# Kernel tuning notes

Measured on AMD Instinct MI355X. Metric: run time of the kernel, lower is better.

The kernel has to match this reference:

```python
import jax, jax.numpy as jnp
import numpy as np

# dims: batch, sentences, p/q/a token lens, choices, hidden, selected sentences
B, N, P, Q, A, M, L, K = 32, 32, 64, 32, 24, 4, 768, 2
EPS = 1e-8


def _normalize(x):
    n = jnp.linalg.norm(x, axis=-1, keepdims=True)
    return x / jnp.maximum(n, EPS)


def setup_inputs() -> dict:
    key = jax.random.key(0)
    ks = jax.random.split(key, 16)
    w = lambda k, shape: jax.random.normal(k, shape, jnp.float32) * 0.02
    return {
        "H_p": jax.random.normal(ks[0], (B, N * P, L), jnp.float32),
        "H_q": jax.random.normal(ks[1], (B, Q, L), jnp.float32),
        "H_a": jax.random.normal(ks[2], (B, M * A, L), jnp.float32),
        "W5": w(ks[3], (L, L)),
        "W6": w(ks[4], ((M - 1) * L, L)),
        "W7": w(ks[5], (L, L)),
        "W8": w(ks[6], (L, L)),
        "b8": jnp.zeros((L,), jnp.float32),
        "W9": w(ks[7], (L, L)),
        "W10": w(ks[8], (L, L)),
        "W11": w(ks[9], (L, L)),
        "W12": w(ks[10], (L, L)),
        "W13": w(ks[11], (L, L)),
        "W14": w(ks[12], (L, L)),
        "b14": jnp.zeros((L,), jnp.float32),
        "V": w(ks[13], (3 * L, 1)),
    }


def reference(H_p, H_q, H_a, W5, W6, W7, W8, b8, W9, W10, W11, W12, W13, W14, b14, V):
    Bq = H_q.shape[0]
    Hp = H_p.reshape(Bq, N, P, L)   # (B, N, p, l)
    Ha = H_a.reshape(Bq, M, A, L)   # (B, m, a, l)

    # --- passage sentence selection (cosine scoring) ---
    # The torch code materializes O(B*m*N*a*p*l) repeated tensors; the math is just
    # pairwise cosine similarity -> max over passage tokens -> mean over a/q tokens.
    Pn, An, Qn = _normalize(Hp), _normalize(Ha), _normalize(H_q)
    sim_pa = jnp.einsum('bnpl,bmal->bmnap', Pn, An)  # (B, m, N, a, p)
    score_a = sim_pa.max(-1).mean(-1).sum(1)          # max over p, mean over a, sum over m -> (B, N)
    sim_pq = jnp.einsum('bnpl,bql->bnqp', Pn, Qn)     # (B, N, q, p)
    score_q = sim_pq.max(-1).mean(-1)                 # (B, N)
    score = score_a + score_q
    top_idx = jnp.argsort(-score, axis=-1)[:, :K]     # descending, top-K sentences
    H_p_s = jnp.take_along_axis(Hp, top_idx[:, :, None, None], axis=1).reshape(Bq, K * P, L)

    # --- answer option interaction ---
    H_o = []
    for i in range(M):
        Hi = Ha[:, i]                                  # (B, a, l)
        cache1 = Hi @ W5
        hats = []
        for j in range(M):
            if j != i:
                Hj = Ha[:, j]
                G = jax.nn.softmax(jnp.einsum('bal,bkl->bak', cache1, Hj), axis=-1)
                hats.append(jax.nn.relu(jnp.einsum('bak,bkl->bal', G, Hj)))
        bar = jnp.concatenate(hats, axis=-1) @ W6      # (B, a, l)
        g = jax.nn.sigmoid(bar @ W7 + bar @ W8 + b8)
        H_o.append(g * Hi + (1.0 - g) * bar)
    H_o = jnp.stack(H_o, axis=1)                       # (B, m, a, l)

    # --- bidirectional matching ---
    def match(Hx, Hy, Gxy_left, Gyx_left):
        Gxy = jax.nn.softmax(jnp.einsum('bxl,byl->bxy', Gxy_left, Hy), axis=-1)
        Gyx = jax.nn.softmax(jnp.einsum('byl,bxl->byx', Gyx_left, Hx), axis=-1)
        Ex = jnp.einsum('bxy,byl->bxl', Gxy, Hy)
        Ey = jnp.einsum('byx,bxl->byl', Gyx, Hx)
        Sxy = jax.nn.relu(Ex @ W11).max(1)             # (B, l)
        Syx = jax.nn.relu(Ey @ W12).max(1)             # (B, l)
        g = jax.nn.sigmoid(Sxy @ W13 + Syx @ W14 + b14)
        return g * Sxy + (1.0 - g) * Syx

    cache1 = H_p_s @ W9
    cache2 = H_q @ W9
    cache3 = H_q @ W10
    M_pq = match(H_p_s, H_q, cache1, cache3)
    C = []
    for i in range(M):
        Hoi = H_o[:, i]
        cache4 = Hoi @ W10
        M_po = match(H_p_s, Hoi, cache1, cache4)
        M_qo = match(H_q, Hoi, cache2, cache4)
        C.append(jnp.concatenate([M_pq, M_po, M_qo], axis=-1))
    C = jnp.stack(C, axis=1)                           # (B, m, 3l)
    logits = (C @ V).squeeze(-1)                       # (B, m)
    return jax.nn.log_softmax(logits, axis=-1)
```

## Files before the change

### kernel.cpp

```cpp
#include <hip/hip_runtime.h>
#include <math.h>


typedef __bf16 bf16x8 __attribute__((ext_vector_type(8)));
typedef float f32x4 __attribute__((ext_vector_type(4)));

__global__ __launch_bounds__(256) void prep_kernel(
    const float* __restrict__ W5, const float* __restrict__ W6,
    const float* __restrict__ W7, const float* __restrict__ W8,
    const float* __restrict__ W9, const float* __restrict__ W10,
    const float* __restrict__ W11, const float* __restrict__ W12,
    const float* __restrict__ W13, const float* __restrict__ W14,
    __bf16* __restrict__ W5t_h, __bf16* __restrict__ W5t_l,
    __bf16* __restrict__ WsQT_h, __bf16* __restrict__ WsQT_l,
    __bf16* __restrict__ W6t_h, __bf16* __restrict__ W6t_l,
    __bf16* __restrict__ W1112T, __bf16* __restrict__ W78t,
    __bf16* __restrict__ W1314t) {
    __shared__ float T[32][33];
    int blk = blockIdx.x;
    int job, rel;
    if (blk < 576) { job = 0; rel = blk; }
    else if (blk < 1728) { job = 1; rel = blk - 576; }
    else if (blk < 3456) { job = 2; rel = blk - 1728; }
    else if (blk < 4608) { job = 3; rel = blk - 3456; }
    else if (blk < 5184) { job = 4; rel = blk - 4608; }
    else { job = 5; rel = blk - 5184; }
    int KT = (job == 2) ? 72 : (job == 5) ? 48 : 24;
    int Kdim = KT * 32;
    int ntile = rel / KT, ktile = rel - ntile * KT;
    int k0 = ktile * 32, n0 = ntile * 32;
    int t = threadIdx.x, tx = t & 31, ty = t >> 5;
#pragma unroll
    for (int s = 0; s < 4; s++) {
        int k = k0 + ty + 8 * s;
        int n = n0 + tx;
        float v;
        switch (job) {
            case 0: v = W5[(long)k * 768 + n]; break;
            case 1: v = (n < 768) ? W9[(long)k * 768 + n] : W10[(long)k * 768 + n - 768]; break;
            case 2: v = W6[(long)k * 768 + n]; break;
            case 3: v = (n < 768) ? W11[(long)k * 768 + n] : W12[(long)k * 768 + n - 768]; break;
            case 4: v = W7[(long)k * 768 + n] + W8[(long)k * 768 + n]; break;
            default: v = (k < 768) ? W13[(long)k * 768 + n] : W14[(long)(k - 768) * 768 + n]; break;
        }
        T[ty + 8 * s][tx] = v;
    }
    __syncthreads();
#pragma unroll
    for (int s = 0; s < 4; s++) {
        int n = n0 + ty + 8 * s;
        int k = k0 + tx;
        float v = T[tx][ty + 8 * s];
        long o = (long)n * Kdim + k;
        __bf16 h = (__bf16)v;
        switch (job) {
            case 0: W5t_h[o] = h; W5t_l[o] = (__bf16)(v - (float)h); break;
            case 1: WsQT_h[o] = h; WsQT_l[o] = (__bf16)(v - (float)h); break;
            case 2: W6t_h[o] = h; W6t_l[o] = (__bf16)(v - (float)h); break;
            case 3: W1112T[o] = h; break;
            case 4: W78t[o] = h; break;
            default: W1314t[o] = h; break;
        }
    }
}

__global__ __launch_bounds__(256) void cvt2n_kernel(const float* __restrict__ src,
                                                    __bf16* __restrict__ h, __bf16* __restrict__ l,
                                                    float* __restrict__ rn) {
    long row = blockIdx.x;
    int t = threadIdx.x;
    const float* sr = src + row * 768;
    float ss = 0.f;
#pragma unroll
    for (int i = 0; i < 3; i++) {
        int idx = t + i * 256;
        float v = sr[idx];
        __bf16 hv = (__bf16)v;
        h[row * 768 + idx] = hv; l[row * 768 + idx] = (__bf16)(v - (float)hv);
        ss += v * v;
    }
    for (int o = 32; o; o >>= 1) ss += __shfl_xor(ss, o);
    __shared__ float red[4];
    if ((t & 63) == 0) red[t >> 6] = ss;
    __syncthreads();
    if (t == 0) rn[row] = 1.f / fmaxf(sqrtf(red[0] + red[1] + red[2] + red[3]), 1e-8f);
}

__global__ __launch_bounds__(256) void simmax_kernel(
    const float* __restrict__ Hp,
    const __bf16* __restrict__ Ha_h, const __bf16* __restrict__ Ha_l,
    const __bf16* __restrict__ Hq_h, const __bf16* __restrict__ Hq_l,
    const float* __restrict__ ra, const float* __restrict__ rq,
    float* __restrict__ amax) {
    constexpr int LDT = 72;
    __shared__ alignas(16) __bf16 Ah[64 * LDT];
    __shared__ alignas(16) __bf16 Al[64 * LDT];
    __shared__ alignas(16) __bf16 Bh[128 * LDT];
    __shared__ alignas(16) __bf16 Bl[128 * LDT];
    __shared__ float rp_lds[64];
    __shared__ float wred[4][128];
    int b = blockIdx.x >> 5, n = blockIdx.x & 31;
    int t = threadIdx.x;
    const float* Ap = Hp + ((long)b * 2048 + n * 64) * 768;
    int srow = t >> 2, kq = (t & 3) << 4;
    int brow = t >> 1, kh = (t & 1) << 5;
    const __bf16 *Bsh, *Bsl;
    if (brow < 96) {
        Bsh = Ha_h + (long)b * 73728 + (long)brow * 768;
        Bsl = Ha_l + (long)b * 73728 + (long)brow * 768;
    } else {
        Bsh = Hq_h + (long)b * 24576 + (long)(brow - 96) * 768;
        Bsl = Hq_l + (long)b * 24576 + (long)(brow - 96) * 768;
    }
    int w = t >> 6, l = t & 63;
    int fr = l & 15, g = l >> 4;
    int wr = w << 4;
    f32x4 acc[8] = {};
    float ss = 0.f;
    const float* Arow = Ap + (long)srow * 768 + kq;
    float4 av0, av1, av2, av3;
    bf16x8 vbh0, vbh1, vbh2, vbh3, vbl0, vbl1, vbl2, vbl3;
    auto LOADS = [&](int k0) {
        av0 = *(const float4*)(Arow + k0 + 0);
        av1 = *(const float4*)(Arow + k0 + 4);
        av2 = *(const float4*)(Arow + k0 + 8);
        av3 = *(const float4*)(Arow + k0 + 12);
        vbh0 = *(const bf16x8*)(Bsh + k0 + kh);
        vbh1 = *(const bf16x8*)(Bsh + k0 + kh + 8);
        vbh2 = *(const bf16x8*)(Bsh + k0 + kh + 16);
        vbh3 = *(const bf16x8*)(Bsh + k0 + kh + 24);
        vbl0 = *(const bf16x8*)(Bsl + k0 + kh);
        vbl1 = *(const bf16x8*)(Bsl + k0 + kh + 8);
        vbl2 = *(const bf16x8*)(Bsl + k0 + kh + 16);
        vbl3 = *(const bf16x8*)(Bsl + k0 + kh + 24);
    };
    LOADS(0);
    for (int k0 = 0; k0 < 768; k0 += 64) {
        float va[16];
        *(float4*)(va + 0) = av0; *(float4*)(va + 4) = av1;
        *(float4*)(va + 8) = av2; *(float4*)(va + 12) = av3;
        bf16x8 h0, h1, l0, l1;
#pragma unroll
        for (int i = 0; i < 8; i++) {
            float v = va[i]; __bf16 hv = (__bf16)v;
            h0[i] = hv; l0[i] = (__bf16)(v - (float)hv); ss += v * v;
            v = va[8 + i]; hv = (__bf16)v;
            h1[i] = hv; l1[i] = (__bf16)(v - (float)hv); ss += v * v;
        }
        bf16x8 sbh0 = vbh0, sbh1 = vbh1, sbh2 = vbh2, sbh3 = vbh3;
        bf16x8 sbl0 = vbl0, sbl1 = vbl1, sbl2 = vbl2, sbl3 = vbl3;
        __syncthreads();
        *(bf16x8*)(&Ah[srow * LDT + kq]) = h0;
        *(bf16x8*)(&Ah[srow * LDT + kq + 8]) = h1;
        *(bf16x8*)(&Al[srow * LDT + kq]) = l0;
        *(bf16x8*)(&Al[srow * LDT + kq + 8]) = l1;
        *(bf16x8*)(&Bh[brow * LDT + kh]) = sbh0;
        *(bf16x8*)(&Bh[brow * LDT + kh + 8]) = sbh1;
        *(bf16x8*)(&Bh[brow * LDT + kh + 16]) = sbh2;
        *(bf16x8*)(&Bh[brow * LDT + kh + 24]) = sbh3;
        *(bf16x8*)(&Bl[brow * LDT + kh]) = sbl0;
        *(bf16x8*)(&Bl[brow * LDT + kh + 8]) = sbl1;
        *(bf16x8*)(&Bl[brow * LDT + kh + 16]) = sbl2;
        *(bf16x8*)(&Bl[brow * LDT + kh + 24]) = sbl3;
        if (k0 + 64 < 768) LOADS(k0 + 64);
        __syncthreads();
#pragma unroll
        for (int sub = 0; sub < 2; sub++) {
            int kb = sub * 32 + g * 8;
            bf16x8 fah = *(const bf16x8*)(&Ah[(wr + fr) * LDT + kb]);
            bf16x8 fal = *(const bf16x8*)(&Al[(wr + fr) * LDT + kb]);
#pragma unroll
            for (int c = 0; c < 8; c++) {
                bf16x8 fbh = *(const bf16x8*)(&Bh[(c * 16 + fr) * LDT + kb]);
                bf16x8 fbl = *(const bf16x8*)(&Bl[(c * 16 + fr) * LDT + kb]);
                acc[c] = __builtin_amdgcn_mfma_f32_16x16x32_bf16(fah, fbh, acc[c], 0, 0, 0);
                acc[c] = __builtin_amdgcn_mfma_f32_16x16x32_bf16(fah, fbl, acc[c], 0, 0, 0);
                acc[c] = __builtin_amdgcn_mfma_f32_16x16x32_bf16(fal, fbh, acc[c], 0, 0, 0);
            }
        }
    }
    ss += __shfl_xor(ss, 1);
    ss += __shfl_xor(ss, 2);
    if ((t & 3) == 0) rp_lds[srow] = 1.f / fmaxf(sqrtf(ss), 1e-8f);
    __syncthreads();
    float rpv[4];
#pragma unroll
    for (int r = 0; r < 4; r++) rpv[r] = rp_lds[wr + g * 4 + r];
#pragma unroll
    for (int c = 0; c < 8; c++) {
        float mx = acc[c][0] * rpv[0];
        mx = fmaxf(mx, acc[c][1] * rpv[1]);
        mx = fmaxf(mx, acc[c][2] * rpv[2]);
        mx = fmaxf(mx, acc[c][3] * rpv[3]);
        mx = fmaxf(mx, __shfl_xor(mx, 16));
        mx = fmaxf(mx, __shfl_xor(mx, 32));
        if (g == 0) wred[w][c * 16 + fr] = mx;
    }
    __syncthreads();
    if (t < 128) {
        float m = fmaxf(fmaxf(wred[0][t], wred[1][t]), fmaxf(wred[2][t], wred[3][t]));
        float rc = (t < 96) ? ra[b * 96 + t] : rq[b * 32 + (t - 96)];
        amax[((long)b * 32 + n) * 128 + t] = m * rc;
    }
}

__global__ void score_top2_kernel(const float* __restrict__ amax, int* __restrict__ idx) {
    int b = blockIdx.x, t = threadIdx.x;
    __shared__ float sc[32];
    if (t < 32) {
        const float* am = amax + ((long)b * 32 + t) * 128;
        float sa = 0.f, sq = 0.f;
        for (int c = 0; c < 96; c++) sa += am[c];
        for (int c = 96; c < 128; c++) sq += am[c];
        sc[t] = sa / 24.f + sq / 32.f;
    }
    __syncthreads();
    if (t == 0) {
        float m0 = -1e30f; int i0 = 0;
        for (int n = 0; n < 32; n++) if (sc[n] > m0) { m0 = sc[n]; i0 = n; }
        float m1 = -1e30f; int i1 = 0;
        for (int n = 0; n < 32; n++) if (n != i0 && sc[n] > m1) { m1 = sc[n]; i1 = n; }
        idx[b * 2] = i0; idx[b * 2 + 1] = i1;
    }
}

__global__ void gather_kernel(const float* __restrict__ Hp, const int* __restrict__ idx,
                              __bf16* __restrict__ Hps_h, __bf16* __restrict__ Hps_l) {
    long i = (long)blockIdx.x * 256 + threadIdx.x;
    if (i >= (long)32 * 128 * 768) return;
    int l = (int)(i % 768);
    long r = i / 768;
    int x = (int)(r % 128); int b = (int)(r / 128);
    int k = x >> 6, p = x & 63;
    int n = idx[b * 2 + k];
    float v = Hp[((long)b * 2048 + n * 64 + p) * 768 + l];
    __bf16 h = (__bf16)v; Hps_h[i] = h; Hps_l[i] = (__bf16)(v - (float)h);
}

template <int BIASF, int BOUT>
__global__ __launch_bounds__(256) void mgemm_kernel(
    const __bf16* __restrict__ A, int Kdim, int Mtot,
    const __bf16* __restrict__ Wt, const float* __restrict__ bias,
    float* __restrict__ C, int ldc, __bf16* __restrict__ Cb) {
    constexpr int LDT = 80;
    __shared__ alignas(16) __bf16 As[64 * LDT];
    __shared__ alignas(16) __bf16 Bs[64 * LDT];
    int t = threadIdx.x;
    int rowBase = blockIdx.x << 6, colBase = blockIdx.y << 6;
    int srow = t >> 2, skof = (t & 3) << 3;
    int arow = rowBase + srow;
    bool aok = arow < Mtot;
    const __bf16* Ap = A + (long)(aok ? arow : rowBase) * Kdim + skof;
    const __bf16* Wp = Wt + (long)(colBase + srow) * Kdim + skof;
    int w = t >> 6, l = t & 63;
    int wr = (w >> 1) << 5, wc = (w & 1) << 5;
    int fr = l & 15, g = l >> 4;
    f32x4 acc[2][2] = {};
    int nk = Kdim >> 6;
    bf16x8 a0, a1, w0, w1;
    auto LOADM = [&]() {
        a0 = *(const bf16x8*)(Ap); a1 = *(const bf16x8*)(Ap + 32);
        w0 = *(const bf16x8*)(Wp); w1 = *(const bf16x8*)(Wp + 32);
        Ap += 64; Wp += 64;
    };
    LOADM();
    for (int ks = 0; ks < nk; ks++) {
        __syncthreads();
        *(bf16x8*)(&As[srow * LDT + skof]) = a0;
        *(bf16x8*)(&As[srow * LDT + 32 + skof]) = a1;
        *(bf16x8*)(&Bs[srow * LDT + skof]) = w0;
        *(bf16x8*)(&Bs[srow * LDT + 32 + skof]) = w1;
        if (ks + 1 < nk) LOADM();
        __syncthreads();
#pragma unroll
        for (int sub = 0; sub < 2; sub++) {
            int ko = sub * 32 + g * 8;
            bf16x8 fa0 = *(const bf16x8*)(&As[(wr + fr) * LDT + ko]);
            bf16x8 fa1 = *(const bf16x8*)(&As[(wr + 16 + fr) * LDT + ko]);
            bf16x8 fb0 = *(const bf16x8*)(&Bs[(wc + fr) * LDT + ko]);
            bf16x8 fb1 = *(const bf16x8*)(&Bs[(wc + 16 + fr) * LDT + ko]);
            acc[0][0] = __builtin_amdgcn_mfma_f32_16x16x32_bf16(fa0, fb0, acc[0][0], 0, 0, 0);
            acc[0][1] = __builtin_amdgcn_mfma_f32_16x16x32_bf16(fa0, fb1, acc[0][1], 0, 0, 0);
            acc[1][0] = __builtin_amdgcn_mfma_f32_16x16x32_bf16(fa1, fb0, acc[1][0], 0, 0, 0);
            acc[1][1] = __builtin_amdgcn_mfma_f32_16x16x32_bf16(fa1, fb1, acc[1][1], 0, 0, 0);
        }
    }
#pragma unroll
    for (int fi = 0; fi < 2; fi++)
#pragma unroll
    for (int fj = 0; fj < 2; fj++)
#pragma unroll
    for (int r = 0; r < 4; r++) {
        int row = rowBase + wr + fi * 16 + g * 4 + r;
        int col = colBase + wc + fj * 16 + (l & 15);
        if (row < Mtot) {
            float v = acc[fi][fj][r];
            if (BIASF) v += bias[col];
            if (BOUT == 0) C[(long)row * ldc + col] = v;
            else Cb[(long)row * ldc + col] = (__bf16)v;
        }
    }
}

__global__ __launch_bounds__(256) void mgemm_gate_kernel(
    const __bf16* __restrict__ A, const __bf16* __restrict__ Wt, const float* __restrict__ bias,
    const float* __restrict__ HaF, const float* __restrict__ barF,
    __bf16* __restrict__ Ho_h, __bf16* __restrict__ Ho_l) {
    constexpr int LDT = 80;
    constexpr int Kdim = 768;
    __shared__ alignas(16) __bf16 As[64 * LDT];
    __shared__ alignas(16) __bf16 Bs[64 * LDT];
    int t = threadIdx.x;
    int rowBase = blockIdx.x << 6, colBase = blockIdx.y << 6;
    int srow = t >> 2, skof = (t & 3) << 3;
    const __bf16* Ap = A + (long)(rowBase + srow) * Kdim + skof;
    const __bf16* Wp = Wt + (long)(colBase + srow) * Kdim + skof;
    int w = t >> 6, l = t & 63;
    int wr = (w >> 1) << 5, wc = (w & 1) << 5;
    int fr = l & 15, g = l >> 4;
    f32x4 acc[2][2] = {};
    bf16x8 a0, a1, w0, w1;
    auto LOADM = [&]() {
        a0 = *(const bf16x8*)(Ap); a1 = *(const bf16x8*)(Ap + 32);
        w0 = *(const bf16x8*)(Wp); w1 = *(const bf16x8*)(Wp + 32);
        Ap += 64; Wp += 64;
    };
    LOADM();
    for (int ks = 0; ks < 12; ks++) {
        __syncthreads();
        *(bf16x8*)(&As[srow * LDT + skof]) = a0;
        *(bf16x8*)(&As[srow * LDT + 32 + skof]) = a1;
        *(bf16x8*)(&Bs[srow * LDT + skof]) = w0;
        *(bf16x8*)(&Bs[srow * LDT + 32 + skof]) = w1;
        if (ks + 1 < 12) LOADM();
        __syncthreads();
#pragma unroll
        for (int sub = 0; sub < 2; sub++) {
            int ko = sub * 32 + g * 8;
            bf16x8 fa0 = *(const bf16x8*)(&As[(wr + fr) * LDT + ko]);
            bf16x8 fa1 = *(const bf16x8*)(&As[(wr + 16 + fr) * LDT + ko]);
            bf16x8 fb0 = *(const bf16x8*)(&Bs[(wc + fr) * LDT + ko]);
            bf16x8 fb1 = *(const bf16x8*)(&Bs[(wc + 16 + fr) * LDT + ko]);
            acc[0][0] = __builtin_amdgcn_mfma_f32_16x16x32_bf16(fa0, fb0, acc[0][0], 0, 0, 0);
            acc[0][1] = __builtin_amdgcn_mfma_f32_16x16x32_bf16(fa0, fb1, acc[0][1], 0, 0, 0);
            acc[1][0] = __builtin_amdgcn_mfma_f32_16x16x32_bf16(fa1, fb0, acc[1][0], 0, 0, 0);
            acc[1][1] = __builtin_amdgcn_mfma_f32_16x16x32_bf16(fa1, fb1, acc[1][1], 0, 0, 0);
        }
    }
#pragma unroll
    for (int fi = 0; fi < 2; fi++)
#pragma unroll
    for (int fj = 0; fj < 2; fj++)
#pragma unroll
    for (int r = 0; r < 4; r++) {
        int row = rowBase + wr + fi * 16 + g * 4 + r;
        int col = colBase + wc + fj * 16 + (l & 15);
        float v = acc[fi][fj][r] + bias[col];
        float gt = 1.f / (1.f + expf(-v));
        long o = (long)row * 768 + col;
        float hv = gt * HaF[o] + (1.f - gt) * barF[o];
        __bf16 hb = (__bf16)hv;
        Ho_h[o] = hb; Ho_l[o] = (__bf16)(hv - (float)hb);
    }
}

template <int OUT>
__global__ __launch_bounds__(256) void mgemm3_kernel(
    const __bf16* __restrict__ Ah, const __bf16* __restrict__ Al, int Kdim, int Mtot,
    const __bf16* __restrict__ Wh, const __bf16* __restrict__ Wl,
    float* __restrict__ C, int ldc, __bf16* __restrict__ Ch, __bf16* __restrict__ Cl) {
    constexpr int LDT = 80;
    __shared__ alignas(16) __bf16 Ahs[64 * LDT];
    __shared__ alignas(16) __bf16 Als[64 * LDT];
    __shared__ alignas(16) __bf16 Bhs[64 * LDT];
    __shared__ alignas(16) __bf16 Bls[64 * LDT];
    int t = threadIdx.x;
    int rowBase = blockIdx.x << 6, colBase = blockIdx.y << 6;
    int srow = t >> 2, skof = (t & 3) << 3;
    int arow = rowBase + srow;
    bool aok = arow < Mtot;
    long aoff = (long)(aok ? arow : rowBase) * Kdim + skof;
    long woff = (long)(colBase + srow) * Kdim + skof;
    const __bf16* Aph = Ah + aoff;
    const __bf16* Apl = Al + aoff;
    const __bf16* Wph = Wh + woff;
    const __bf16* Wpl = Wl + woff;
    int w = t >> 6, l = t & 63;
    int wr = (w >> 1) << 5, wc = (w & 1) << 5;
    int fr = l & 15, g = l >> 4;
    f32x4 acc[2][2] = {};
    int nk = Kdim >> 6;
    bf16x8 ah0, ah1, al0, al1, wh0, wh1, wl0, wl1;
    auto LOADM = [&]() {
        ah0 = *(const bf16x8*)(Aph); ah1 = *(const bf16x8*)(Aph + 32);
        al0 = *(const bf16x8*)(Apl); al1 = *(const bf16x8*)(Apl + 32);
        wh0 = *(const bf16x8*)(Wph); wh1 = *(const bf16x8*)(Wph + 32);
        wl0 = *(const bf16x8*)(Wpl); wl1 = *(const bf16x8*)(Wpl + 32);
        Aph += 64; Apl += 64; Wph += 64; Wpl += 64;
    };
    LOADM();
    for (int ks = 0; ks < nk; ks++) {
        __syncthreads();
        *(bf16x8*)(&Ahs[srow * LDT + skof]) = ah0; *(bf16x8*)(&Ahs[srow * LDT + 32 + skof]) = ah1;
        *(bf16x8*)(&Als[srow * LDT + skof]) = al0; *(bf16x8*)(&Als[srow * LDT + 32 + skof]) = al1;
        *(bf16x8*)(&Bhs[srow * LDT + skof]) = wh0; *(bf16x8*)(&Bhs[srow * LDT + 32 + skof]) = wh1;
        *(bf16x8*)(&Bls[srow * LDT + skof]) = wl0; *(bf16x8*)(&Bls[srow * LDT + 32 + skof]) = wl1;
        if (ks + 1 < nk) LOADM();
        __syncthreads();
#pragma unroll
        for (int sub = 0; sub < 2; sub++) {
            int ko = sub * 32 + g * 8;
            bf16x8 fah[2], fal[2], fbh[2], fbl[2];
            fah[0] = *(const bf16x8*)(&Ahs[(wr + fr) * LDT + ko]);
            fah[1] = *(const bf16x8*)(&Ahs[(wr + 16 + fr) * LDT + ko]);
            fal[0] = *(const bf16x8*)(&Als[(wr + fr) * LDT + ko]);
            fal[1] = *(const bf16x8*)(&Als[(wr + 16 + fr) * LDT + ko]);
            fbh[0] = *(const bf16x8*)(&Bhs[(wc + fr) * LDT + ko]);
            fbh[1] = *(const bf16x8*)(&Bhs[(wc + 16 + fr) * LDT + ko]);
            fbl[0] = *(const bf16x8*)(&Bls[(wc + fr) * LDT + ko]);
            fbl[1] = *(const bf16x8*)(&Bls[(wc + 16 + fr) * LDT + ko]);
#pragma unroll
            for (int i = 0; i < 2; i++)
#pragma unroll
            for (int j = 0; j < 2; j++) {
                acc[i][j] = __builtin_amdgcn_mfma_f32_16x16x32_bf16(fah[i], fbh[j], acc[i][j], 0, 0, 0);
                acc[i][j] = __builtin_amdgcn_mfma_f32_16x16x32_bf16(fah[i], fbl[j], acc[i][j], 0, 0, 0);
                acc[i][j] = __builtin_amdgcn_mfma_f32_16x16x32_bf16(fal[i], fbh[j], acc[i][j], 0, 0, 0);
            }
        }
    }
#pragma unroll
    for (int fi = 0; fi < 2; fi++)
#pragma unroll
    for (int fj = 0; fj < 2; fj++)
#pragma unroll
    for (int r = 0; r < 4; r++) {
        int row = rowBase + wr + fi * 16 + g * 4 + r;
        int col = colBase + wc + fj * 16 + (l & 15);
        if (row < Mtot) {
            float v = acc[fi][fj][r];
            long o = (long)row * ldc + col;
            if (OUT == 0) { C[o] = v; }
            else if (OUT == 1) { C[o] = v; Ch[o] = (__bf16)v; }
            else {
                __bf16 h = (__bf16)v;
                Ch[o] = h; Cl[o] = (__bf16)(v - (float)h);
            }
        }
    }
}

struct PXSeg { const __bf16 *Ah, *Al, *Wh, *Wl; __bf16 *Ch, *Cl; int Mtot, ldc, gx; };
struct PXArgs { PXSeg s[3]; };

__global__ __launch_bounds__(256) void projx_kernel(PXArgs args) {
    constexpr int LDT = 80;
    __shared__ alignas(16) __bf16 Ahs[64 * LDT];
    __shared__ alignas(16) __bf16 Als[64 * LDT];
    __shared__ alignas(16) __bf16 Bhs[64 * LDT];
    __shared__ alignas(16) __bf16 Bls[64 * LDT];
    int bid = blockIdx.x;
    int seg = (bid < 576) ? 0 : (bid < 960) ? 1 : 2;
    int rel = bid - ((seg == 0) ? 0 : (seg == 1) ? 576 : 960);
    PXSeg sg = args.s[seg];
    int rowBase = (rel % sg.gx) << 6, colBase = (rel / sg.gx) << 6;
    int t = threadIdx.x;
    int srow = t >> 2, skof = (t & 3) << 3;
    long aoff = (long)(rowBase + srow) * 768 + skof;
    long woff = (long)(colBase + srow) * 768 + skof;
    const __bf16* Aph = sg.Ah + aoff;
    const __bf16* Apl = sg.Al + aoff;
    const __bf16* Wph = sg.Wh + woff;
    const __bf16* Wpl = sg.Wl + woff;
    int w = t >> 6, l = t & 63;
    int wr = (w >> 1) << 5, wc = (w & 1) << 5;
    int fr = l & 15, g = l >> 4;
    f32x4 acc[2][2] = {};
    bf16x8 ah0, ah1, al0, al1, wh0, wh1, wl0, wl1;
    auto LOADM = [&]() {
        ah0 = *(const bf16x8*)(Aph); ah1 = *(const bf16x8*)(Aph + 32);
        al0 = *(const bf16x8*)(Apl); al1 = *(const bf16x8*)(Apl + 32);
        wh0 = *(const bf16x8*)(Wph); wh1 = *(const bf16x8*)(Wph + 32);
        wl0 = *(const bf16x8*)(Wpl); wl1 = *(const bf16x8*)(Wpl + 32);
        Aph += 64; Apl += 64; Wph += 64; Wpl += 64;
    };
    LOADM();
    for (int ks = 0; ks < 12; ks++) {
        __syncthreads();
        *(bf16x8*)(&Ahs[srow * LDT + skof]) = ah0; *(bf16x8*)(&Ahs[srow * LDT + 32 + skof]) = ah1;
        *(bf16x8*)(&Als[srow * LDT + skof]) = al0; *(bf16x8*)(&Als[srow * LDT + 32 + skof]) = al1;
        *(bf16x8*)(&Bhs[srow * LDT + skof]) = wh0; *(bf16x8*)(&Bhs[srow * LDT + 32 + skof]) = wh1;
        *(bf16x8*)(&Bls[srow * LDT + skof]) = wl0; *(bf16x8*)(&Bls[srow * LDT + 32 + skof]) = wl1;
        if (ks + 1 < 12) LOADM();
        __syncthreads();
#pragma unroll
        for (int sub = 0; sub < 2; sub++) {
            int ko = sub * 32 + g * 8;
            bf16x8 fah[2], fal[2], fbh[2], fbl[2];
            fah[0] = *(const bf16x8*)(&Ahs[(wr + fr) * LDT + ko]);
            fah[1] = *(const bf16x8*)(&Ahs[(wr + 16 + fr) * LDT + ko]);
            fal[0] = *(const bf16x8*)(&Als[(wr + fr) * LDT + ko]);
            fal[1] = *(const bf16x8*)(&Als[(wr + 16 + fr) * LDT + ko]);
            fbh[0] = *(const bf16x8*)(&Bhs[(wc + fr) * LDT + ko]);
            fbh[1] = *(const bf16x8*)(&Bhs[(wc + 16 + fr) * LDT + ko]);
            fbl[0] = *(const bf16x8*)(&Bls[(wc + fr) * LDT + ko]);
            fbl[1] = *(const bf16x8*)(&Bls[(wc + 16 + fr) * LDT + ko]);
#pragma unroll
            for (int i = 0; i < 2; i++)
#pragma unroll
            for (int j = 0; j < 2; j++) {
                acc[i][j] = __builtin_amdgcn_mfma_f32_16x16x32_bf16(fah[i], fbh[j], acc[i][j], 0, 0, 0);
                acc[i][j] = __builtin_amdgcn_mfma_f32_16x16x32_bf16(fah[i], fbl[j], acc[i][j], 0, 0, 0);
                acc[i][j] = __builtin_amdgcn_mfma_f32_16x16x32_bf16(fal[i], fbh[j], acc[i][j], 0, 0, 0);
            }
        }
    }
#pragma unroll
    for (int fi = 0; fi < 2; fi++)
#pragma unroll
    for (int fj = 0; fj < 2; fj++)
#pragma unroll
    for (int r = 0; r < 4; r++) {
        int row = rowBase + wr + fi * 16 + g * 4 + r;
        int col = colBase + wc + fj * 16 + (l & 15);
        if (row < sg.Mtot) {
            float v = acc[fi][fj][r];
            long o = (long)row * sg.ldc + col;
            __bf16 h = (__bf16)v;
            sg.Ch[o] = h; sg.Cl[o] = (__bf16)(v - (float)h);
        }
    }
}

struct PPSeg { const __bf16 *A, *Wt; __bf16* Cb; int Mtot, ldc, gx; };
struct PPArgs { PPSeg s[2]; };

__global__ __launch_bounds__(256) void projp_kernel(PPArgs args) {
    constexpr int LDT = 80;
    __shared__ alignas(16) __bf16 As[64 * LDT];
    __shared__ alignas(16) __bf16 Bs[64 * LDT];
    int bid = blockIdx.x;
    int seg = (bid < 384) ? 0 : 1;
    int rel = bid - ((seg == 0) ? 0 : 384);
    PPSeg sg = args.s[seg];
    int rowBase = (rel % sg.gx) << 6, colBase = (rel / sg.gx) << 6;
    int t = threadIdx.x;
    int srow = t >> 2, skof = (t & 3) << 3;
    const __bf16* Ap = sg.A + (long)(rowBase + srow) * 768 + skof;
    const __bf16* Wp = sg.Wt + (long)(colBase + srow) * 768 + skof;
    int w = t >> 6, l = t & 63;
    int wr = (w >> 1) << 5, wc = (w & 1) << 5;
    int fr = l & 15, g = l >> 4;
    f32x4 acc[2][2] = {};
    bf16x8 a0, a1, w0, w1;
    auto LOADM = [&]() {
        a0 = *(const bf16x8*)(Ap); a1 = *(const bf16x8*)(Ap + 32);
        w0 = *(const bf16x8*)(Wp); w1 = *(const bf16x8*)(Wp + 32);
        Ap += 64; Wp += 64;
    };
    LOADM();
    for (int ks = 0; ks < 12; ks++) {
        __syncthreads();
        *(bf16x8*)(&As[srow * LDT + skof]) = a0;
        *(bf16x8*)(&As[srow * LDT + 32 + skof]) = a1;
        *(bf16x8*)(&Bs[srow * LDT + skof]) = w0;
        *(bf16x8*)(&Bs[srow * LDT + 32 + skof]) = w1;
        if (ks + 1 < 12) LOADM();
        __syncthreads();
#pragma unroll
        for (int sub = 0; sub < 2; sub++) {
            int ko = sub * 32 + g * 8;
            bf16x8 fa0 = *(const bf16x8*)(&As[(wr + fr) * LDT + ko]);
            bf16x8 fa1 = *(const bf16x8*)(&As[(wr + 16 + fr) * LDT + ko]);
            bf16x8 fb0 = *(const bf16x8*)(&Bs[(wc + fr) * LDT + ko]);
            bf16x8 fb1 = *(const bf16x8*)(&Bs[(wc + 16 + fr) * LDT + ko]);
            acc[0][0] = __builtin_amdgcn_mfma_f32_16x16x32_bf16(fa0, fb0, acc[0][0], 0, 0, 0);
            acc[0][1] = __builtin_amdgcn_mfma_f32_16x16x32_bf16(fa0, fb1, acc[0][1], 0, 0, 0);
            acc[1][0] = __builtin_amdgcn_mfma_f32_16x16x32_bf16(fa1, fb0, acc[1][0], 0, 0, 0);
            acc[1][1] = __builtin_amdgcn_mfma_f32_16x16x32_bf16(fa1, fb1, acc[1][1], 0, 0, 0);
        }
    }
#pragma unroll
    for (int fi = 0; fi < 2; fi++)
#pragma unroll
    for (int fj = 0; fj < 2; fj++)
#pragma unroll
    for (int r = 0; r < 4; r++) {
        int row = rowBase + wr + fi * 16 + g * 4 + r;
        int col = colBase + wc + fj * 16 + (l & 15);
        if (row < sg.Mtot)
            sg.Cb[(long)row * sg.ldc + col] = (__bf16)acc[fi][fj][r];
    }
}

struct QHSeg {
    const __bf16 *GLh, *GLl, *HYh, *HYl;
    __bf16 *outH, *outL;
    long glB, hyB, oB;
};
struct QHArgs { QHSeg s[12]; };

__global__ __launch_bounds__(256) void qkh_kernel(QHArgs args) {
    constexpr int X = 24, Y = 24, XR = 32, YR = 32, LDT = 72;
    constexpr int YRp = YR + 1;
    constexpr int Ck = 32, Cpad = 40;
    constexpr int scPad = (XR * YRp * 4 + 15) & ~15;
    constexpr int btSz = 2 * 64 * Cpad * 2;
    constexpr int gOff = btSz;
    __shared__ alignas(16) char POOL[gOff + 2 * XR * Cpad * 2];
    __shared__ alignas(16) char POOL2[18432 - (gOff + 2 * XR * Cpad * 2)];
    (void)POOL2;
    __bf16* Ah_ = (__bf16*)POOL;
    __bf16* Al_ = Ah_ + XR * LDT;
    int seg = blockIdx.x >> 5, b = blockIdx.x & 31;
    QHSeg sg = args.s[seg];
    int t = threadIdx.x;
    __bf16* Bh_ = Ah_ + 2 * XR * LDT;
    __bf16* Bl_ = Bh_ + YR * LDT;
    float* sc   = (float*)POOL;
    float* invr = (float*)(POOL + scPad);
    __bf16* Bth = (__bf16*)POOL;
    __bf16* Btl = Bth + 64 * Cpad;
    __bf16* Gh  = (__bf16*)(POOL + gOff);
    __bf16* Gl  = Gh + XR * Cpad;
    int w = t >> 6, l = t & 63, fr = l & 15, g = l >> 4;
    const __bf16* GLbh = sg.GLh + (long)b * sg.glB;
    const __bf16* GLbl = sg.GLl + (long)b * sg.glB;
    const __bf16* HYbh = sg.HYh + (long)b * sg.hyB;
    const __bf16* HYbl = sg.HYl + (long)b * sg.hyB;
    f32x4 acc;
#pragma unroll
    for (int r = 0; r < 4; r++) acc[r] = 0.f;
    for (int k0 = 0; k0 < 768; k0 += 64) {
        __syncthreads();
        for (int v = t; v < (XR + YR) * 16; v += 256) {
            int row = v >> 4, sub = v & 15, hl = sub >> 3, k8 = (sub & 7) << 3;
            bf16x8 val = {};
            __bf16* dst;
            if (row < XR) {
                if (row < X)
                    val = *(const bf16x8*)((hl ? GLbl : GLbh) + (long)row * 768 + k0 + k8);
                dst = (hl ? Al_ : Ah_) + row * LDT + k8;
            } else {
                int r2 = row - XR;
                if (r2 < Y)
                    val = *(const bf16x8*)((hl ? HYbl : HYbh) + (long)r2 * 768 + k0 + k8);
                dst = (hl ? Bl_ : Bh_) + r2 * LDT + k8;
            }
            *(bf16x8*)dst = val;
        }
        __syncthreads();
#pragma unroll
        for (int sub = 0; sub < 2; sub++) {
            int kb = sub * 32 + g * 8;
            int xm = w >> 1, yc = w & 1;
            bf16x8 fah = *(const bf16x8*)(&Ah_[(xm * 16 + fr) * LDT + kb]);
            bf16x8 fal = *(const bf16x8*)(&Al_[(xm * 16 + fr) * LDT + kb]);
            bf16x8 fbh = *(const bf16x8*)(&Bh_[(yc * 16 + fr) * LDT + kb]);
            bf16x8 fbl = *(const bf16x8*)(&Bl_[(yc * 16 + fr) * LDT + kb]);
            acc = __builtin_amdgcn_mfma_f32_16x16x32_bf16(fah, fbh, acc, 0, 0, 0);
            acc = __builtin_amdgcn_mfma_f32_16x16x32_bf16(fah, fbl, acc, 0, 0, 0);
            acc = __builtin_amdgcn_mfma_f32_16x16x32_bf16(fal, fbh, acc, 0, 0, 0);
        }
    }
    __syncthreads();
    {
        int xm = w >> 1, yc = w & 1;
#pragma unroll
        for (int r = 0; r < 4; r++)
            sc[(xm * 16 + g * 4 + r) * YRp + yc * 16 + fr] = acc[r];
    }
    __syncthreads();
    {
        constexpr int TPR = 256 / XR;
        int row = t / TPR, sub = t & (TPR - 1);
        if (row < X) {
            float* sr = sc + row * YRp;
            float m = -1e30f;
            for (int c = sub; c < Y; c += TPR) m = fmaxf(m, sr[c]);
#pragma unroll
            for (int o = 1; o < TPR; o <<= 1) m = fmaxf(m, __shfl_xor(m, o));
            float s = 0.f;
            for (int c = sub; c < Y; c += TPR) { float e = expf(sr[c] - m); sr[c] = e; s += e; }
#pragma unroll
            for (int o = 1; o < TPR; o <<= 1) s += __shfl_xor(s, o);
            if (sub == 0) invr[row] = 1.f / s;
        }
    }
    __syncthreads();
    for (int idx = t; idx < XR * Ck; idx += 256) {
        int r = idx >> 5, c = idx & 31;
        float v = (r < X && c < Y) ? sc[r * YRp + c] * invr[r] : 0.f;
        __bf16 h = (__bf16)v;
        Gh[r * Cpad + c] = h; Gl[r * Cpad + c] = (__bf16)(v - (float)h);
    }
    int bl = t & 63, bc0 = t >> 6;
    for (int n0 = 0; n0 < 768; n0 += 64) {
        __syncthreads();
        for (int c = bc0; c < Ck; c += 4) {
            __bf16 hv = (__bf16)0.f, lv = (__bf16)0.f;
            if (c < Y) { hv = HYbh[(long)c * 768 + n0 + bl]; lv = HYbl[(long)c * 768 + n0 + bl]; }
            Bth[bl * Cpad + c] = hv; Btl[bl * Cpad + c] = lv;
        }
        __syncthreads();
        bf16x8 bh = *(const bf16x8*)(&Bth[(w * 16 + fr) * Cpad + g * 8]);
        bf16x8 blv = *(const bf16x8*)(&Btl[(w * 16 + fr) * Cpad + g * 8]);
        f32x4 a2[2] = {};
#pragma unroll
        for (int m = 0; m < 2; m++) {
            bf16x8 gah = *(const bf16x8*)(&Gh[(m * 16 + fr) * Cpad + g * 8]);
            bf16x8 gal = *(const bf16x8*)(&Gl[(m * 16 + fr) * Cpad + g * 8]);
            a2[m] = __builtin_amdgcn_mfma_f32_16x16x32_bf16(gah, bh, a2[m], 0, 0, 0);
            a2[m] = __builtin_amdgcn_mfma_f32_16x16x32_bf16(gal, bh, a2[m], 0, 0, 0);
            a2[m] = __builtin_amdgcn_mfma_f32_16x16x32_bf16(gah, blv, a2[m], 0, 0, 0);
        }
#pragma unroll
        for (int m = 0; m < 2; m++)
#pragma unroll
        for (int r = 0; r < 4; r++) {
            int row = m * 16 + g * 4 + r;
            if (row < X) {
                float v = fmaxf(a2[m][r], 0.f);
                __bf16 h = (__bf16)v;
                long o = (long)b * sg.oB + (long)row * 2304 + n0 + w * 16 + fr;
                sg.outH[o] = h; sg.outL[o] = (__bf16)(v - (float)h);
            }
        }
    }
}

struct QSSeg {
    const __bf16 *GLh, *GLl, *HYh, *HYl, *B;
    float* outF; __bf16* outH;
    long glB, hyB, bB;
    int ldGL, ldHY, ldB, shape;
};
struct QSArgs { QSSeg s[18]; };

template <int X, int Y>
__device__ __forceinline__ void qks_impl(char* POOL, const QSSeg& sg, int b, int t) {
    constexpr int XR = (X + 15) & ~15;
    constexpr int YR = (Y + 15) & ~15;
    constexpr int LDT = 72;
    constexpr int YC = YR / 16;
    constexpr int F = (XR / 16) * YC;
    constexpr int F4 = F / 4;
    constexpr int YRp = YR + 1;
    constexpr int Rk = XR;
    constexpr int Ck = (Y + 31) & ~31;
    constexpr int Cpad = Ck + 8;
    constexpr int NM = Rk / 16;
    constexpr int scPad = (XR * YRp * 4 + 15) & ~15;
    constexpr int invrEnd = scPad + 512;
    constexpr int btSz = 64 * Cpad * 2;
    constexpr int gOff = ((invrEnd > btSz ? invrEnd : btSz) + 15) & ~15;
    static_assert(gOff + 2 * Rk * Cpad * 2 <= 46080, "pool overflow");
    __bf16* Ah_ = (__bf16*)POOL;
    __bf16* Al_ = Ah_ + XR * LDT;
    __bf16* Bh_ = Ah_ + 2 * XR * LDT;
    __bf16* Bl_ = Bh_ + YR * LDT;
    float* sc   = (float*)POOL;
    float* invr = (float*)(POOL + scPad);
    __bf16* Bt  = (__bf16*)POOL;
    __bf16* Gh  = (__bf16*)(POOL + gOff);
    __bf16* Gl  = Gh + Rk * Cpad;
    int w = t >> 6, l = t & 63, fr = l & 15, g = l >> 4;
    const __bf16* GLbh = sg.GLh + (long)b * sg.glB;
    const __bf16* GLbl = sg.GLl + (long)b * sg.glB;
    const __bf16* HYbh = sg.HYh + (long)b * sg.hyB;
    const __bf16* HYbl = sg.HYl + (long)b * sg.hyB;
    f32x4 acc[F4] = {};
    for (int k0 = 0; k0 < 768; k0 += 64) {
        __syncthreads();
        for (int v = t; v < (XR + YR) * 16; v += 256) {
            int row = v >> 4, sub = v & 15, hl = sub >> 3, k8 = (sub & 7) << 3;
            bf16x8 val = {};
            __bf16* dst;
            if (row < XR) {
                if (row < X)
                    val = *(const bf16x8*)((hl ? GLbl : GLbh) + (long)row * sg.ldGL + k0 + k8);
                dst = (hl ? Al_ : Ah_) + row * LDT + k8;
            } else {
                int r2 = row - XR;
                if (r2 < Y)
                    val = *(const bf16x8*)((hl ? HYbl : HYbh) + (long)r2 * sg.ldHY + k0 + k8);
                dst = (hl ? Bl_ : Bh_) + r2 * LDT + k8;
            }
            *(bf16x8*)dst = val;
        }
        __syncthreads();
#pragma unroll
        for (int sub = 0; sub < 2; sub++) {
            int kb = sub * 32 + g * 8;
#pragma unroll
            for (int ff = 0; ff < F4; ff++) {
                int fidx = w + ff * 4;
                int xm = fidx / YC, yc = fidx % YC;
                bf16x8 fah = *(const bf16x8*)(&Ah_[(xm * 16 + fr) * LDT + kb]);
                bf16x8 fal = *(const bf16x8*)(&Al_[(xm * 16 + fr) * LDT + kb]);
                bf16x8 fbh = *(const bf16x8*)(&Bh_[(yc * 16 + fr) * LDT + kb]);
                bf16x8 fbl = *(const bf16x8*)(&Bl_[(yc * 16 + fr) * LDT + kb]);
                acc[ff] = __builtin_amdgcn_mfma_f32_16x16x32_bf16(fah, fbh, acc[ff], 0, 0, 0);
                acc[ff] = __builtin_amdgcn_mfma_f32_16x16x32_bf16(fah, fbl, acc[ff], 0, 0, 0);
                acc[ff] = __builtin_amdgcn_mfma_f32_16x16x32_bf16(fal, fbh, acc[ff], 0, 0, 0);
            }
        }
    }
    __syncthreads();
#pragma unroll
    for (int ff = 0; ff < F4; ff++) {
        int fidx = w + ff * 4;
        int xm = fidx / YC, yc = fidx % YC;
#pragma unroll
        for (int r = 0; r < 4; r++)
            sc[(xm * 16 + g * 4 + r) * YRp + yc * 16 + fr] = acc[ff][r];
    }
    __syncthreads();
    {
        constexpr int TPR = 256 / XR;
        int row = t / TPR, sub = t & (TPR - 1);
        if (row < X) {
            float* sr = sc + row * YRp;
            float m = -1e30f;
            for (int c = sub; c < Y; c += TPR) m = fmaxf(m, sr[c]);
#pragma unroll
            for (int o = 1; o < TPR; o <<= 1) m = fmaxf(m, __shfl_xor(m, o));
            float s = 0.f;
            for (int c = sub; c < Y; c += TPR) { float e = expf(sr[c] - m); sr[c] = e; s += e; }
#pragma unroll
            for (int o = 1; o < TPR; o <<= 1) s += __shfl_xor(s, o);
            if (sub == 0) invr[row] = 1.f / s;
        }
    }
    __syncthreads();
    for (int idx = t; idx < Rk * Ck; idx += 256) {
        int r = idx / Ck, c = idx - r * Ck;
        float v = (r < X && c < Y) ? sc[r * YRp + c] * invr[r] : 0.f;
        __bf16 h = (__bf16)v;
        Gh[r * Cpad + c] = h; Gl[r * Cpad + c] = (__bf16)(v - (float)h);
    }
    const __bf16* Bb = sg.B + (long)b * sg.bB;
    int bl = t & 63, bc0 = t >> 6;
    for (int n0 = 0; n0 < 768; n0 += 64) {
        __syncthreads();
        for (int c = bc0; c < Ck; c += 4) {
            __bf16 hv = (__bf16)0.f;
            if (c < Y) hv = Bb[(long)c * sg.ldB + n0 + bl];
            Bt[bl * Cpad + c] = hv;
        }
        __syncthreads();
        f32x4 a2[NM] = {};
#pragma unroll
        for (int ks = 0; ks < Ck; ks += 32) {
            bf16x8 bh = *(const bf16x8*)(&Bt[(w * 16 + fr) * Cpad + ks + g * 8]);
#pragma unroll
            for (int m = 0; m < NM; m++) {
                bf16x8 gah = *(const bf16x8*)(&Gh[(m * 16 + fr) * Cpad + ks + g * 8]);
                bf16x8 gal = *(const bf16x8*)(&Gl[(m * 16 + fr) * Cpad + ks + g * 8]);
                a2[m] = __builtin_amdgcn_mfma_f32_16x16x32_bf16(gah, bh, a2[m], 0, 0, 0);
                a2[m] = __builtin_amdgcn_mfma_f32_16x16x32_bf16(gal, bh, a2[m], 0, 0, 0);
            }
        }
        float mx = 0.f;
#pragma unroll
        for (int m = 0; m < NM; m++)
#pragma unroll
            for (int r = 0; r < 4; r++) mx = fmaxf(mx, a2[m][r]);
        mx = fmaxf(mx, __shfl_xor(mx, 16));
        mx = fmaxf(mx, __shfl_xor(mx, 32));
        if (g == 0) {
            int col = n0 + w * 16 + fr;
            sg.outF[(long)b * 1536 + col] = mx;
            sg.outH[(long)b * 1536 + col] = (__bf16)mx;
        }
    }
}

__global__ __launch_bounds__(256) void qks_kernel(QSArgs args) {
    __shared__ alignas(16) char POOL[46080];
    int seg = blockIdx.x >> 5, b = blockIdx.x & 31;
    QSSeg sg = args.s[seg];
    int t = threadIdx.x;
    switch (sg.shape) {
        case 1: qks_impl<128, 32>(POOL, sg, b, t); break;
        case 2: qks_impl<128, 24>(POOL, sg, b, t); break;
        case 3: qks_impl<32, 24>(POOL, sg, b, t); break;
        case 4: qks_impl<24, 32>(POOL, sg, b, t); break;
        case 5: qks_impl<32, 128>(POOL, sg, b, t); break;
        default: qks_impl<24, 128>(POOL, sg, b, t); break;
    }
}

__global__ __launch_bounds__(256) void logits_lsm_kernel(
    const float* __restrict__ S, const float* __restrict__ gts,
    const float* __restrict__ V, float* __restrict__ out) {
    int b = blockIdx.x;
    int t = threadIdx.x, i = t >> 6, lane = t & 63;
    int ms[3] = {0, 1 + i, 5 + i};
    float p = 0.f;
    for (int k = 0; k < 3; k++) {
        int m = ms[k];
        const float* Sr = S + (long)m * 49152 + (long)b * 1536;
        const float* gr = gts + ((long)m * 32 + b) * 768;
        const float* Vr = V + k * 768;
        for (int l = lane; l < 768; l += 64) {
            float g = 1.f / (1.f + expf(-gr[l]));
            p += (g * Sr[l] + (1.f - g) * Sr[768 + l]) * Vr[l];
        }
    }
    for (int o = 32; o; o >>= 1) p += __shfl_xor(p, o);
    __shared__ float lgs[4];
    if (lane == 0) lgs[i] = p;
    __syncthreads();
    if (t == 0) {
        float x0 = lgs[0], x1 = lgs[1], x2 = lgs[2], x3 = lgs[3];
        float m = fmaxf(fmaxf(x0, x1), fmaxf(x2, x3));
        float s = expf(x0 - m) + expf(x1 - m) + expf(x2 - m) + expf(x3 - m);
        float ls = m + logf(s);
        out[b * 4 + 0] = x0 - ls; out[b * 4 + 1] = x1 - ls;
        out[b * 4 + 2] = x2 - ls; out[b * 4 + 3] = x3 - ls;
    }
}

extern "C" void kernel_launch(void* const* d_in, const int* in_sizes, int n_in,
                              void* d_out, int out_size, void* d_ws, size_t ws_size,
                              hipStream_t stream) {
    const float* Hp  = (const float*)d_in[0];
    const float* Hq  = (const float*)d_in[1];
    const float* Ha  = (const float*)d_in[2];
    const float* W5  = (const float*)d_in[3];
    const float* W6  = (const float*)d_in[4];
    const float* W7  = (const float*)d_in[5];
    const float* W8  = (const float*)d_in[6];
    const float* b8  = (const float*)d_in[7];
    const float* W9  = (const float*)d_in[8];
    const float* W10 = (const float*)d_in[9];
    const float* W11 = (const float*)d_in[10];
    const float* W12 = (const float*)d_in[11];
    const float* W13 = (const float*)d_in[12];
    const float* W14 = (const float*)d_in[13];
    const float* b14 = (const float*)d_in[14];
    const float* V   = (const float*)d_in[15];
    float* out = (float*)d_out;
    (void)in_sizes; (void)n_in; (void)out_size; (void)ws_size;

    char* base = (char*)d_ws;
    size_t off = 0;
    auto take = [&](size_t bytes) { char* p = base + off; off += (bytes + 15) & ~15UL; return p; };

    __bf16* W5t_h  = (__bf16*)take(1179648);
    __bf16* W5t_l  = (__bf16*)take(1179648);
    __bf16* WsQT_h = (__bf16*)take(2359296);
    __bf16* WsQT_l = (__bf16*)take(2359296);
    __bf16* W6t_h  = (__bf16*)take(3538944);
    __bf16* W6t_l  = (__bf16*)take(3538944);
    __bf16* W1112T = (__bf16*)take(2359296);
    __bf16* W78t   = (__bf16*)take(1179648);
    __bf16* W1314t = (__bf16*)take(2359296);
    float* ra     = (float*)take(12288);
    float* rq     = (float*)take(4096);
    float* amax   = (float*)take(524288);
    int*   topidx = (int*)take(256);
    __bf16* Ha_h  = (__bf16*)take(4718592);
    __bf16* Ha_l  = (__bf16*)take(4718592);
    __bf16* Hq_h  = (__bf16*)take(1572864);
    __bf16* Hq_l  = (__bf16*)take(1572864);
    __bf16* Hps_h = (__bf16*)take(6291456);
    __bf16* Hps_l = (__bf16*)take(6291456);
    __bf16* C1_h  = (__bf16*)take(4718592);
    __bf16* C1_l  = (__bf16*)take(4718592);
    __bf16* HqS_h = (__bf16*)take(3145728);
    __bf16* HqS_l = (__bf16*)take(3145728);
    __bf16* c1_h  = (__bf16*)take(6291456);
    __bf16* c1_l  = (__bf16*)take(6291456);
    __bf16* c4_h  = (__bf16*)take(4718592);
    __bf16* c4_l  = (__bf16*)take(4718592);
    __bf16* Ho_h  = (__bf16*)take(4718592);
    __bf16* Ho_l  = (__bf16*)take(4718592);
    __bf16* hats_h = (__bf16*)take(14155776);
    __bf16* hats_l = (__bf16*)take(14155776);
    __bf16* bar_h  = (__bf16*)take(4718592);
    __bf16* HqS2_bf   = (__bf16*)take(3145728);
    __bf16* HpsW12_bf = (__bf16*)take(6291456);
    __bf16* HoW11_bf  = (__bf16*)take(4718592);
    __bf16* S_h    = (__bf16*)take(884736);
    float* bar  = (float*)take(9437184);
    float* S    = (float*)take(1769472);
    float* gts  = (float*)take(884736);

    dim3 blk(256);

    prep_kernel<<<6336, blk, 0, stream>>>(W5, W6, W7, W8, W9, W10, W11, W12, W13, W14,
                                          W5t_h, W5t_l, WsQT_h, WsQT_l, W6t_h, W6t_l,
                                          W1112T, W78t, W1314t);
    cvt2n_kernel<<<3072, blk, 0, stream>>>(Ha, Ha_h, Ha_l, ra);
    cvt2n_kernel<<<1024, blk, 0, stream>>>(Hq, Hq_h, Hq_l, rq);

    simmax_kernel<<<1024, blk, 0, stream>>>(Hp, Ha_h, Ha_l, Hq_h, Hq_l, ra, rq, amax);
    score_top2_kernel<<<32, dim3(64), 0, stream>>>(amax, topidx);
    gather_kernel<<<12288, blk, 0, stream>>>(Hp, topidx, Hps_h, Hps_l);

    {
        PXArgs pa{};
        pa.s[0] = { Ha_h, Ha_l, W5t_h, W5t_l, C1_h, C1_l, 3072, 768, 48 };
        pa.s[1] = { Hq_h, Hq_l, WsQT_h, WsQT_l, HqS_h, HqS_l, 1024, 1536, 16 };
        pa.s[2] = { Hps_h, Hps_l, WsQT_h, WsQT_l, c1_h, c1_l, 4096, 768, 64 };
        projx_kernel<<<1728, blk, 0, stream>>>(pa);
    }
    {
        PPArgs pa{};
        pa.s[0] = { Hq_h, W1112T, HqS2_bf, 1024, 1536, 16 };
        pa.s[1] = { Hps_h, W1112T + (long)768 * 768, HpsW12_bf, 4096, 768, 64 };
        projp_kernel<<<1152, blk, 0, stream>>>(pa);
    }

    {
        QHArgs qa{}; int si = 0;
        for (int i = 0; i < 4; i++) {
            int jj = 0;
            for (int j = 0; j < 4; j++) {
                if (j == i) continue;
                QHSeg& s = qa.s[si];
                s.GLh = C1_h + (long)i * 24 * 768; s.GLl = C1_l + (long)i * 24 * 768;
                s.HYh = Ha_h + (long)j * 24 * 768; s.HYl = Ha_l + (long)j * 24 * 768;
                s.outH = hats_h + (long)i * 24 * 2304 + jj * 768;
                s.outL = hats_l + (long)i * 24 * 2304 + jj * 768;
                s.glB = 73728; s.hyB = 73728; s.oB = 221184;
                si++; jj++;
            }
        }
        qkh_kernel<<<12 * 32, blk, 0, stream>>>(qa);
    }
    mgemm3_kernel<1><<<dim3(48, 12), blk, 0, stream>>>(hats_h, hats_l, 2304, 3072, W6t_h, W6t_l, bar, 768, bar_h, nullptr);
    mgemm_gate_kernel<<<dim3(48, 12), blk, 0, stream>>>(bar_h, W78t, b8, Ha, bar, Ho_h, Ho_l);
    mgemm3_kernel<2><<<dim3(48, 12), blk, 0, stream>>>(Ho_h, Ho_l, 768, 3072, WsQT_h + (long)768 * 768, WsQT_l + (long)768 * 768, nullptr, 768, c4_h, c4_l);
    mgemm_kernel<0, 1><<<dim3(48, 12), blk, 0, stream>>>(Ho_h, 768, 3072, W1112T, nullptr, nullptr, 768, HoW11_bf);

    {
        QSArgs qa{};
        auto set = [&](int k, const __bf16* GLh, const __bf16* GLl, long glB, int ldGL,
                       const __bf16* HYh, const __bf16* HYl, long hyB, int ldHY,
                       const __bf16* B, long bB, int ldB,
                       float* oF, __bf16* oH, int shape) {
            QSSeg& s = qa.s[k];
            s.GLh = GLh; s.GLl = GLl; s.HYh = HYh; s.HYl = HYl; s.B = B;
            s.outF = oF; s.outH = oH;
            s.glB = glB; s.hyB = hyB; s.bB = bB;
            s.ldGL = ldGL; s.ldHY = ldHY; s.ldB = ldB; s.shape = shape;
        };
        set(0, c1_h, c1_l, 98304, 768, Hq_h, Hq_l, 24576, 768,
            HqS2_bf, 49152, 1536, S, S_h, 1);
        for (int i = 0; i < 4; i++) {
            set(1 + i, c1_h, c1_l, 98304, 768,
                Ho_h + (long)i * 24 * 768, Ho_l + (long)i * 24 * 768, 73728, 768,
                HoW11_bf + (long)i * 24 * 768, 73728, 768,
                S + (long)(1 + i) * 49152, S_h + (long)(1 + i) * 49152, 2);
            set(5 + i, HqS_h, HqS_l, 49152, 1536,
                Ho_h + (long)i * 24 * 768, Ho_l + (long)i * 24 * 768, 73728, 768,
                HoW11_bf + (long)i * 24 * 768, 73728, 768,
                S + (long)(5 + i) * 49152, S_h + (long)(5 + i) * 49152, 3);
            set(9 + i, c4_h + (long)i * 24 * 768, c4_l + (long)i * 24 * 768, 73728, 768,
                Hq_h, Hq_l, 24576, 768,
                HqS2_bf + 768, 49152, 1536,
                S + (long)(5 + i) * 49152 + 768, S_h + (long)(5 + i) * 49152 + 768, 4);
        }
        set(13, HqS_h + 768, HqS_l + 768, 49152, 1536, Hps_h, Hps_l, 98304, 768,
            HpsW12_bf, 98304, 768, S + 768, S_h + 768, 5);
        for (int i = 0; i < 4; i++)
            set(14 + i, c4_h + (long)i * 24 * 768, c4_l + (long)i * 24 * 768, 73728, 768,
                Hps_h, Hps_l, 98304, 768,
                HpsW12_bf, 98304, 768,
                S + (long)(1 + i) * 49152 + 768, S_h + (long)(1 + i) * 49152 + 768, 6);
        qks_kernel<<<18 * 32, blk, 0, stream>>>(qa);
    }

    mgemm_kernel<1, 0><<<dim3(5, 12), blk, 0, stream>>>(S_h, 1536, 288, W1314t, b14, gts, 768, nullptr);

    logits_lsm_kernel<<<32, blk, 0, stream>>>(S, gts, V, out);
}
```

Baseline: 442.1 us.

## Enlarge projection GEMM tiles to 128x128 with 4x4 MFMA fragments per wave

Replaces the 64x64-tile projection and split-bf16 GEMM kernels with 128x128-tile versions in which each wave computes a 64x64 sub-tile (4x4 MFMA fragments). The aim is more operand reuse per LDS load and less global traffic per output. It also merges the two cvt2n launches into one and simplifies the qkh shared-memory declaration. In exchange there are far fewer blocks (e.g. 144 instead of 576), which can underfill a 256-CU GPU, and register pressure per wave is higher. The row-bounds checks are dropped, so every M must be a multiple of 128.

```diff
diff --git a/kernel.cpp b/kernel.cpp
--- a/kernel.cpp
+++ b/kernel.cpp
@@ -4,6 +4,8 @@
 
 typedef __bf16 bf16x8 __attribute__((ext_vector_type(8)));
 typedef float f32x4 __attribute__((ext_vector_type(4)));
+
+#define MFMA __builtin_amdgcn_mfma_f32_16x16x32_bf16
 
 __global__ __launch_bounds__(256) void prep_kernel(
     const float* __restrict__ W5, const float* __restrict__ W6,
@@ -64,10 +66,15 @@
     }
 }
 
-__global__ __launch_bounds__(256) void cvt2n_kernel(const float* __restrict__ src,
-                                                    __bf16* __restrict__ h, __bf16* __restrict__ l,
-                                                    float* __restrict__ rn) {
+__global__ __launch_bounds__(256) void cvt2n_kernel(
+    const float* __restrict__ Ha, __bf16* __restrict__ Ha_h, __bf16* __restrict__ Ha_l,
+    float* __restrict__ ra,
+    const float* __restrict__ Hq, __bf16* __restrict__ Hq_h, __bf16* __restrict__ Hq_l,
+    float* __restrict__ rq) {
     long row = blockIdx.x;
+    const float* src; __bf16 *h, *l; float* rn;
+    if (row < 3072) { src = Ha; h = Ha_h; l = Ha_l; rn = ra; }
+    else { row -= 3072; src = Hq; h = Hq_h; l = Hq_l; rn = rq; }
     int t = threadIdx.x;
     const float* sr = src + row * 768;
     float ss = 0.f;
@@ -173,9 +180,9 @@
             for (int c = 0; c < 8; c++) {
                 bf16x8 fbh = *(const bf16x8*)(&Bh[(c * 16 + fr) * LDT + kb]);
                 bf16x8 fbl = *(const bf16x8*)(&Bl[(c * 16 + fr) * LDT + kb]);
-                acc[c] = __builtin_amdgcn_mfma_f32_16x16x32_bf16(fah, fbh, acc[c], 0, 0, 0);
-                acc[c] = __builtin_amdgcn_mfma_f32_16x16x32_bf16(fah, fbl, acc[c], 0, 0, 0);
-                acc[c] = __builtin_amdgcn_mfma_f32_16x16x32_bf16(fal, fbh, acc[c], 0, 0, 0);
+                acc[c] = MFMA(fah, fbh, acc[c], 0, 0, 0);
+                acc[c] = MFMA(fah, fbl, acc[c], 0, 0, 0);
+                acc[c] = MFMA(fal, fbh, acc[c], 0, 0, 0);
             }
         }
     }
@@ -235,6 +242,189 @@
     int n = idx[b * 2 + k];
     float v = Hp[((long)b * 2048 + n * 64 + p) * 768 + l];
     __bf16 h = (__bf16)v; Hps_h[i] = h; Hps_l[i] = (__bf16)(v - (float)h);
+}
+
+template <int OUT>
+__device__ __forceinline__ void mg3b_body(
+    const __bf16* __restrict__ Ah, const __bf16* __restrict__ Al, int Kdim,
+    const __bf16* __restrict__ Wh, const __bf16* __restrict__ Wl,
+    float* __restrict__ C, int ldc, __bf16* __restrict__ Ch, __bf16* __restrict__ Cl,
+    int rowBase, int colBase, int t,
+    __bf16* Ahs, __bf16* Als, __bf16* Bhs, __bf16* Bls) {
+    constexpr int LDT = 40;
+    int srow = t >> 1, skof = (t & 1) << 4;
+    long aoff = (long)(rowBase + srow) * Kdim + skof;
+    long woff = (long)(colBase + srow) * Kdim + skof;
+    const __bf16* Aph = Ah + aoff;
+    const __bf16* Apl = Al + aoff;
+    const __bf16* Wph = Wh + woff;
+    const __bf16* Wpl = Wl + woff;
+    int w = t >> 6, l = t & 63;
+    int wr = (w >> 1) << 6, wc = (w & 1) << 6;
+    int fr = l & 15, g = l >> 4;
+    f32x4 acc[4][4] = {};
+    int nk = Kdim >> 5;
+    bf16x8 rah0, rah1, ral0, ral1, rwh0, rwh1, rwl0, rwl1;
+    auto LOADM = [&]() {
+        rah0 = *(const bf16x8*)(Aph); rah1 = *(const bf16x8*)(Aph + 8);
+        ral0 = *(const bf16x8*)(Apl); ral1 = *(const bf16x8*)(Apl + 8);
+        rwh0 = *(const bf16x8*)(Wph); rwh1 = *(const bf16x8*)(Wph + 8);
+        rwl0 = *(const bf16x8*)(Wpl); rwl1 = *(const bf16x8*)(Wpl + 8);
+        Aph += 32; Apl += 32; Wph += 32; Wpl += 32;
+    };
+    LOADM();
+    for (int ks = 0; ks < nk; ks++) {
+        __syncthreads();
+        *(bf16x8*)(&Ahs[srow * LDT + skof]) = rah0; *(bf16x8*)(&Ahs[srow * LDT + skof + 8]) = rah1;
+        *(bf16x8*)(&Als[srow * LDT + skof]) = ral0; *(bf16x8*)(&Als[srow * LDT + skof + 8]) = ral1;
+        *(bf16x8*)(&Bhs[srow * LDT + skof]) = rwh0; *(bf16x8*)(&Bhs[srow * LDT + skof + 8]) = rwh1;
+        *(bf16x8*)(&Bls[srow * LDT + skof]) = rwl0; *(bf16x8*)(&Bls[srow * LDT + skof + 8]) = rwl1;
+        if (ks + 1 < nk) LOADM();
+        __syncthreads();
+        int kb = g * 8;
+        bf16x8 fah[4], fal[4], fbh[4], fbl[4];
+#pragma unroll
+        for (int i = 0; i < 4; i++) {
+            fah[i] = *(const bf16x8*)(&Ahs[(wr + i * 16 + fr) * LDT + kb]);
+            fal[i] = *(const bf16x8*)(&Als[(wr + i * 16 + fr) * LDT + kb]);
+            fbh[i] = *(const bf16x8*)(&Bhs[(wc + i * 16 + fr) * LDT + kb]);
+            fbl[i] = *(const bf16x8*)(&Bls[(wc + i * 16 + fr) * LDT + kb]);
+        }
+#pragma unroll
+        for (int i = 0; i < 4; i++)
+#pragma unroll
+        for (int j = 0; j < 4; j++) {
+            acc[i][j] = MFMA(fah[i], fbh[j], acc[i][j], 0, 0, 0);
+            acc[i][j] = MFMA(fah[i], fbl[j], acc[i][j], 0, 0, 0);
+            acc[i][j] = MFMA(fal[i], fbh[j], acc[i][j], 0, 0, 0);
+        }
+    }
+#pragma unroll
+    for (int fi = 0; fi < 4; fi++)
+#pragma unroll
+    for (int fj = 0; fj < 4; fj++)
+#pragma unroll
+    for (int r = 0; r < 4; r++) {
+        int row = rowBase + wr + fi * 16 + g * 4 + r;
+        int col = colBase + wc + fj * 16 + fr;
+        float v = acc[fi][fj][r];
+        long o = (long)row * ldc + col;
+        if (OUT == 1) { C[o] = v; Ch[o] = (__bf16)v; }
+        else {
+            __bf16 h = (__bf16)v;
+            Ch[o] = h; Cl[o] = (__bf16)(v - (float)h);
+        }
+    }
+}
+
+template <int OUT>
+__global__ __launch_bounds__(256) void mgemm3b_kernel(
+    const __bf16* __restrict__ Ah, const __bf16* __restrict__ Al, int Kdim,
+    const __bf16* __restrict__ Wh, const __bf16* __restrict__ Wl,
+    float* __restrict__ C, int ldc, __bf16* __restrict__ Ch, __bf16* __restrict__ Cl) {
+    __shared__ alignas(16) __bf16 Ahs[128 * 40];
+    __shared__ alignas(16) __bf16 Als[128 * 40];
+    __shared__ alignas(16) __bf16 Bhs[128 * 40];
+    __shared__ alignas(16) __bf16 Bls[128 * 40];
+    mg3b_body<OUT>(Ah, Al, Kdim, Wh, Wl, C, ldc, Ch, Cl,
+                   blockIdx.x << 7, blockIdx.y << 7, threadIdx.x, Ahs, Als, Bhs, Bls);
+}
+
+struct PXSeg { const __bf16 *Ah, *Al, *Wh, *Wl; __bf16 *Ch, *Cl; int ldc, gx; };
+struct PXArgs { PXSeg s[3]; };
+
+__global__ __launch_bounds__(256) void projxb_kernel(PXArgs args) {
+    __shared__ alignas(16) __bf16 Ahs[128 * 40];
+    __shared__ alignas(16) __bf16 Als[128 * 40];
+    __shared__ alignas(16) __bf16 Bhs[128 * 40];
+    __shared__ alignas(16) __bf16 Bls[128 * 40];
+    int bid = blockIdx.x;
+    int seg = (bid < 144) ? 0 : (bid < 240) ? 1 : 2;
+    int rel = bid - ((seg == 0) ? 0 : (seg == 1) ? 144 : 240);
+    PXSeg sg = args.s[seg];
+    int rowBase = (rel % sg.gx) << 7, colBase = (rel / sg.gx) << 7;
+    mg3b_body<2>(sg.Ah, sg.Al, 768, sg.Wh, sg.Wl, nullptr, sg.ldc, sg.Ch, sg.Cl,
+                 rowBase, colBase, threadIdx.x, Ahs, Als, Bhs, Bls);
+}
+
+__device__ __forceinline__ void mgb_body(
+    const __bf16* __restrict__ A, int Kdim, const __bf16* __restrict__ Wt,
+    __bf16* __restrict__ Cb, int ldc,
+    int rowBase, int colBase, int t, __bf16* As, __bf16* Bs) {
+    constexpr int LDT = 72;
+    int srow = t >> 1, skof = (t & 1) << 5;
+    const __bf16* Ap = A + (long)(rowBase + srow) * Kdim + skof;
+    const __bf16* Wp = Wt + (long)(colBase + srow) * Kdim + skof;
+    int w = t >> 6, l = t & 63;
+    int wr = (w >> 1) << 6, wc = (w & 1) << 6;
+    int fr = l & 15, g = l >> 4;
+    f32x4 acc[4][4] = {};
+    int nk = Kdim >> 6;
+    bf16x8 ra0, ra1, ra2, ra3, rw0, rw1, rw2, rw3;
+    auto LOADM = [&]() {
+        ra0 = *(const bf16x8*)(Ap);      ra1 = *(const bf16x8*)(Ap + 8);
+        ra2 = *(const bf16x8*)(Ap + 16); ra3 = *(const bf16x8*)(Ap + 24);
+        rw0 = *(const bf16x8*)(Wp);      rw1 = *(const bf16x8*)(Wp + 8);
+        rw2 = *(const bf16x8*)(Wp + 16); rw3 = *(const bf16x8*)(Wp + 24);
+        Ap += 64; Wp += 64;
+    };
+    LOADM();
+    for (int ks = 0; ks < nk; ks++) {
+        __syncthreads();
+        *(bf16x8*)(&As[srow * LDT + skof]) = ra0;      *(bf16x8*)(&As[srow * LDT + skof + 8]) = ra1;
+        *(bf16x8*)(&As[srow * LDT + skof + 16]) = ra2; *(bf16x8*)(&As[srow * LDT + skof + 24]) = ra3;
+        *(bf16x8*)(&Bs[srow * LDT + skof]) = rw0;      *(bf16x8*)(&Bs[srow * LDT + skof + 8]) = rw1;
+        *(bf16x8*)(&Bs[srow * LDT + skof + 16]) = rw2; *(bf16x8*)(&Bs[srow * LDT + skof + 24]) = rw3;
+        if (ks + 1 < nk) LOADM();
+        __syncthreads();
+#pragma unroll
+        for (int sub = 0; sub < 2; sub++) {
+            int kb = sub * 32 + g * 8;
+            bf16x8 fa[4], fb[4];
+#pragma unroll
+            for (int i = 0; i < 4; i++) {
+                fa[i] = *(const bf16x8*)(&As[(wr + i * 16 + fr) * LDT + kb]);
+                fb[i] = *(const bf16x8*)(&Bs[(wc + i * 16 + fr) * LDT + kb]);
+            }
+#pragma unroll
+            for (int i = 0; i < 4; i++)
+#pragma unroll
+            for (int j = 0; j < 4; j++)
+                acc[i][j] = MFMA(fa[i], fb[j], acc[i][j], 0, 0, 0);
+        }
+    }
+#pragma unroll
+    for (int fi = 0; fi < 4; fi++)
+#pragma unroll
+    for (int fj = 0; fj < 4; fj++)
+#pragma unroll
+    for (int r = 0; r < 4; r++) {
+        int row = rowBase + wr + fi * 16 + g * 4 + r;
+        int col = colBase + wc + fj * 16 + fr;
+        Cb[(long)row * ldc + col] = (__bf16)acc[fi][fj][r];
+    }
+}
+
+__global__ __launch_bounds__(256) void mgemmb_kernel(
+    const __bf16* __restrict__ A, int Kdim, const __bf16* __restrict__ Wt,
+    __bf16* __restrict__ Cb, int ldc) {
+    __shared__ alignas(16) __bf16 As[128 * 72];
+    __shared__ alignas(16) __bf16 Bs[128 * 72];
+    mgb_body(A, Kdim, Wt, Cb, ldc, blockIdx.x << 7, blockIdx.y << 7, threadIdx.x, As, Bs);
+}
+
+struct PPSeg { const __bf16 *A, *Wt; __bf16* Cb; int ldc, gx; };
+struct PPArgs { PPSeg s[2]; };
+
+__global__ __launch_bounds__(256) void projpb_kernel(PPArgs args) {
+    __shared__ alignas(16) __bf16 As[128 * 72];
+    __shared__ alignas(16) __bf16 Bs[128 * 72];
+    int bid = blockIdx.x;
+    int seg = (bid < 96) ? 0 : 1;
+    int rel = bid - ((seg == 0) ? 0 : 96);
+    PPSeg sg = args.s[seg];
+    int rowBase = (rel % sg.gx) << 7, colBase = (rel / sg.gx) << 7;
+    mgb_body(sg.A, 768, sg.Wt, sg.Cb, sg.ldc, rowBase, colBase, threadIdx.x, As, Bs);
 }
 
 template <int BIASF, int BOUT>
@@ -279,10 +469,10 @@
             bf16x8 fa1 = *(const bf16x8*)(&As[(wr + 16 + fr) * LDT + ko]);
             bf16x8 fb0 = *(const bf16x8*)(&Bs[(wc + fr) * LDT + ko]);
             bf16x8 fb1 = *(const bf16x8*)(&Bs[(wc + 16 + fr) * LDT + ko]);
-            acc[0][0] = __builtin_amdgcn_mfma_f32_16x16x32_bf16(fa0, fb0, acc[0][0], 0, 0, 0);
-            acc[0][1] = __builtin_amdgcn_mfma_f32_16x16x32_bf16(fa0, fb1, acc[0][1], 0, 0, 0);
-            acc[1][0] = __builtin_amdgcn_mfma_f32_16x16x32_bf16(fa1, fb0, acc[1][0], 0, 0, 0);
-            acc[1][1] = __builtin_amdgcn_mfma_f32_16x16x32_bf16(fa1, fb1, acc[1][1], 0, 0, 0);
+            acc[0][0] = MFMA(fa0, fb0, acc[0][0], 0, 0, 0);
+            acc[0][1] = MFMA(fa0, fb1, acc[0][1], 0, 0, 0);
+            acc[1][0] = MFMA(fa1, fb0, acc[1][0], 0, 0, 0);
+            acc[1][1] = MFMA(fa1, fb1, acc[1][1], 0, 0, 0);
         }
     }
 #pragma unroll
@@ -341,10 +531,10 @@
             bf16x8 fa1 = *(const bf16x8*)(&As[(wr + 16 + fr) * LDT + ko]);
             bf16x8 fb0 = *(const bf16x8*)(&Bs[(wc + fr) * LDT + ko]);
             bf16x8 fb1 = *(const bf16x8*)(&Bs[(wc + 16 + fr) * LDT + ko]);
-            acc[0][0] = __builtin_amdgcn_mfma_f32_16x16x32_bf16(fa0, fb0, acc[0][0], 0, 0, 0);
-            acc[0][1] = __builtin_amdgcn_mfma_f32_16x16x32_bf16(fa0, fb1, acc[0][1], 0, 0, 0);
-            acc[1][0] = __builtin_amdgcn_mfma_f32_16x16x32_bf16(fa1, fb0, acc[1][0], 0, 0, 0);
-            acc[1][1] = __builtin_amdgcn_mfma_f32_16x16x32_bf16(fa1, fb1, acc[1][1], 0, 0, 0);
+            acc[0][0] = MFMA(fa0, fb0, acc[0][0], 0, 0, 0);
+            acc[0][1] = MFMA(fa0, fb1, acc[0][1], 0, 0, 0);
+            acc[1][0] = MFMA(fa1, fb0, acc[1][0], 0, 0, 0);
+            acc[1][1] = MFMA(fa1, fb1, acc[1][1], 0, 0, 0);
         }
     }
 #pragma unroll
@@ -364,235 +554,6 @@
     }
 }
 
-template <int OUT>
-__global__ __launch_bounds__(256) void mgemm3_kernel(
-    const __bf16* __restrict__ Ah, const __bf16* __restrict__ Al, int Kdim, int Mtot,
-    const __bf16* __restrict__ Wh, const __bf16* __restrict__ Wl,
-    float* __restrict__ C, int ldc, __bf16* __restrict__ Ch, __bf16* __restrict__ Cl) {
-    constexpr int LDT = 80;
-    __shared__ alignas(16) __bf16 Ahs[64 * LDT];
-    __shared__ alignas(16) __bf16 Als[64 * LDT];
-    __shared__ alignas(16) __bf16 Bhs[64 * LDT];
-    __shared__ alignas(16) __bf16 Bls[64 * LDT];
-    int t = threadIdx.x;
-    int rowBase = blockIdx.x << 6, colBase = blockIdx.y << 6;
-    int srow = t >> 2, skof = (t & 3) << 3;
-    int arow = rowBase + srow;
-    bool aok = arow < Mtot;
-    long aoff = (long)(aok ? arow : rowBase) * Kdim + skof;
-    long woff = (long)(colBase + srow) * Kdim + skof;
-    const __bf16* Aph = Ah + aoff;
-    const __bf16* Apl = Al + aoff;
-    const __bf16* Wph = Wh + woff;
-    const __bf16* Wpl = Wl + woff;
-    int w = t >> 6, l = t & 63;
-    int wr = (w >> 1) << 5, wc = (w & 1) << 5;
-    int fr = l & 15, g = l >> 4;
-    f32x4 acc[2][2] = {};
-    int nk = Kdim >> 6;
-    bf16x8 ah0, ah1, al0, al1, wh0, wh1, wl0, wl1;
-    auto LOADM = [&]() {
-        ah0 = *(const bf16x8*)(Aph); ah1 = *(const bf16x8*)(Aph + 32);
-        al0 = *(const bf16x8*)(Apl); al1 = *(const bf16x8*)(Apl + 32);
-        wh0 = *(const bf16x8*)(Wph); wh1 = *(const bf16x8*)(Wph + 32);
-        wl0 = *(const bf16x8*)(Wpl); wl1 = *(const bf16x8*)(Wpl + 32);
-        Aph += 64; Apl += 64; Wph += 64; Wpl += 64;
-    };
-    LOADM();
-    for (int ks = 0; ks < nk; ks++) {
-        __syncthreads();
-        *(bf16x8*)(&Ahs[srow * LDT + skof]) = ah0; *(bf16x8*)(&Ahs[srow * LDT + 32 + skof]) = ah1;
-        *(bf16x8*)(&Als[srow * LDT + skof]) = al0; *(bf16x8*)(&Als[srow * LDT + 32 + skof]) = al1;
-        *(bf16x8*)(&Bhs[srow * LDT + skof]) = wh0; *(bf16x8*)(&Bhs[srow * LDT + 32 + skof]) = wh1;
-        *(bf16x8*)(&Bls[srow * LDT + skof]) = wl0; *(bf16x8*)(&Bls[srow * LDT + 32 + skof]) = wl1;
-        if (ks + 1 < nk) LOADM();
-        __syncthreads();
-#pragma unroll
-        for (int sub = 0; sub < 2; sub++) {
-            int ko = sub * 32 + g * 8;
-            bf16x8 fah[2], fal[2], fbh[2], fbl[2];
-            fah[0] = *(const bf16x8*)(&Ahs[(wr + fr) * LDT + ko]);
-            fah[1] = *(const bf16x8*)(&Ahs[(wr + 16 + fr) * LDT + ko]);
-            fal[0] = *(const bf16x8*)(&Als[(wr + fr) * LDT + ko]);
-            fal[1] = *(const bf16x8*)(&Als[(wr + 16 + fr) * LDT + ko]);
-            fbh[0] = *(const bf16x8*)(&Bhs[(wc + fr) * LDT + ko]);
-            fbh[1] = *(const bf16x8*)(&Bhs[(wc + 16 + fr) * LDT + ko]);
-            fbl[0] = *(const bf16x8*)(&Bls[(wc + fr) * LDT + ko]);
-            fbl[1] = *(const bf16x8*)(&Bls[(wc + 16 + fr) * LDT + ko]);
-#pragma unroll
-            for (int i = 0; i < 2; i++)
-#pragma unroll
-            for (int j = 0; j < 2; j++) {
-                acc[i][j] = __builtin_amdgcn_mfma_f32_16x16x32_bf16(fah[i], fbh[j], acc[i][j], 0, 0, 0);
-                acc[i][j] = __builtin_amdgcn_mfma_f32_16x16x32_bf16(fah[i], fbl[j], acc[i][j], 0, 0, 0);
-                acc[i][j] = __builtin_amdgcn_mfma_f32_16x16x32_bf16(fal[i], fbh[j], acc[i][j], 0, 0, 0);
-            }
-        }
-    }
-#pragma unroll
-    for (int fi = 0; fi < 2; fi++)
-#pragma unroll
-    for (int fj = 0; fj < 2; fj++)
-#pragma unroll
-    for (int r = 0; r < 4; r++) {
-        int row = rowBase + wr + fi * 16 + g * 4 + r;
-        int col = colBase + wc + fj * 16 + (l & 15);
-        if (row < Mtot) {
-            float v = acc[fi][fj][r];
-            long o = (long)row * ldc + col;
-            if (OUT == 0) { C[o] = v; }
-            else if (OUT == 1) { C[o] = v; Ch[o] = (__bf16)v; }
-            else {
-                __bf16 h = (__bf16)v;
-                Ch[o] = h; Cl[o] = (__bf16)(v - (float)h);
-            }
-        }
-    }
-}
-
-struct PXSeg { const __bf16 *Ah, *Al, *Wh, *Wl; __bf16 *Ch, *Cl; int Mtot, ldc, gx; };
-struct PXArgs { PXSeg s[3]; };
-
-__global__ __launch_bounds__(256) void projx_kernel(PXArgs args) {
-    constexpr int LDT = 80;
-    __shared__ alignas(16) __bf16 Ahs[64 * LDT];
-    __shared__ alignas(16) __bf16 Als[64 * LDT];
-    __shared__ alignas(16) __bf16 Bhs[64 * LDT];
-    __shared__ alignas(16) __bf16 Bls[64 * LDT];
-    int bid = blockIdx.x;
-    int seg = (bid < 576) ? 0 : (bid < 960) ? 1 : 2;
-    int rel = bid - ((seg == 0) ? 0 : (seg == 1) ? 576 : 960);
-    PXSeg sg = args.s[seg];
-    int rowBase = (rel % sg.gx) << 6, colBase = (rel / sg.gx) << 6;
-    int t = threadIdx.x;
-    int srow = t >> 2, skof = (t & 3) << 3;
-    long aoff = (long)(rowBase + srow) * 768 + skof;
-    long woff = (long)(colBase + srow) * 768 + skof;
-    const __bf16* Aph = sg.Ah + aoff;
-    const __bf16* Apl = sg.Al + aoff;
-    const __bf16* Wph = sg.Wh + woff;
-    const __bf16* Wpl = sg.Wl + woff;
-    int w = t >> 6, l = t & 63;
-    int wr = (w >> 1) << 5, wc = (w & 1) << 5;
-    int fr = l & 15, g = l >> 4;
-    f32x4 acc[2][2] = {};
-    bf16x8 ah0, ah1, al0, al1, wh0, wh1, wl0, wl1;
-    auto LOADM = [&]() {
-        ah0 = *(const bf16x8*)(Aph); ah1 = *(const bf16x8*)(Aph + 32);
-        al0 = *(const bf16x8*)(Apl); al1 = *(const bf16x8*)(Apl + 32);
-        wh0 = *(const bf16x8*)(Wph); wh1 = *(const bf16x8*)(Wph + 32);
-        wl0 = *(const bf16x8*)(Wpl); wl1 = *(const bf16x8*)(Wpl + 32);
-        Aph += 64; Apl += 64; Wph += 64; Wpl += 64;
-    };
-    LOADM();
-    for (int ks = 0; ks < 12; ks++) {
-        __syncthreads();
-        *(bf16x8*)(&Ahs[srow * LDT + skof]) = ah0; *(bf16x8*)(&Ahs[srow * LDT + 32 + skof]) = ah1;
-        *(bf16x8*)(&Als[srow * LDT + skof]) = al0; *(bf16x8*)(&Als[srow * LDT + 32 + skof]) = al1;
-        *(bf16x8*)(&Bhs[srow * LDT + skof]) = wh0; *(bf16x8*)(&Bhs[srow * LDT + 32 + skof]) = wh1;
-        *(bf16x8*)(&Bls[srow * LDT + skof]) = wl0; *(bf16x8*)(&Bls[srow * LDT + 32 + skof]) = wl1;
-        if (ks + 1 < 12) LOADM();
-        __syncthreads();
-#pragma unroll
-        for (int sub = 0; sub < 2; sub++) {
-            int ko = sub * 32 + g * 8;
-            bf16x8 fah[2], fal[2], fbh[2], fbl[2];
-            fah[0] = *(const bf16x8*)(&Ahs[(wr + fr) * LDT + ko]);
-            fah[1] = *(const bf16x8*)(&Ahs[(wr + 16 + fr) * LDT + ko]);
-            fal[0] = *(const bf16x8*)(&Als[(wr + fr) * LDT + ko]);
-            fal[1] = *(const bf16x8*)(&Als[(wr + 16 + fr) * LDT + ko]);
-            fbh[0] = *(const bf16x8*)(&Bhs[(wc + fr) * LDT + ko]);
-            fbh[1] = *(const bf16x8*)(&Bhs[(wc + 16 + fr) * LDT + ko]);
-            fbl[0] = *(const bf16x8*)(&Bls[(wc + fr) * LDT + ko]);
-            fbl[1] = *(const bf16x8*)(&Bls[(wc + 16 + fr) * LDT + ko]);
-#pragma unroll
-            for (int i = 0; i < 2; i++)
-#pragma unroll
-            for (int j = 0; j < 2; j++) {
-                acc[i][j] = __builtin_amdgcn_mfma_f32_16x16x32_bf16(fah[i], fbh[j], acc[i][j], 0, 0, 0);
-                acc[i][j] = __builtin_amdgcn_mfma_f32_16x16x32_bf16(fah[i], fbl[j], acc[i][j], 0, 0, 0);
-                acc[i][j] = __builtin_amdgcn_mfma_f32_16x16x32_bf16(fal[i], fbh[j], acc[i][j], 0, 0, 0);
-            }
-        }
-    }
-#pragma unroll
-    for (int fi = 0; fi < 2; fi++)
-#pragma unroll
-    for (int fj = 0; fj < 2; fj++)
-#pragma unroll
-    for (int r = 0; r < 4; r++) {
-        int row = rowBase + wr + fi * 16 + g * 4 + r;
-        int col = colBase + wc + fj * 16 + (l & 15);
-        if (row < sg.Mtot) {
-            float v = acc[fi][fj][r];
-            long o = (long)row * sg.ldc + col;
-            __bf16 h = (__bf16)v;
-            sg.Ch[o] = h; sg.Cl[o] = (__bf16)(v - (float)h);
-        }
-    }
-}
-
-struct PPSeg { const __bf16 *A, *Wt; __bf16* Cb; int Mtot, ldc, gx; };
-struct PPArgs { PPSeg s[2]; };
-
-__global__ __launch_bounds__(256) void projp_kernel(PPArgs args) {
-    constexpr int LDT = 80;
-    __shared__ alignas(16) __bf16 As[64 * LDT];
-    __shared__ alignas(16) __bf16 Bs[64 * LDT];
-    int bid = blockIdx.x;
-    int seg = (bid < 384) ? 0 : 1;
-    int rel = bid - ((seg == 0) ? 0 : 384);
-    PPSeg sg = args.s[seg];
-    int rowBase = (rel % sg.gx) << 6, colBase = (rel / sg.gx) << 6;
-    int t = threadIdx.x;
-    int srow = t >> 2, skof = (t & 3) << 3;
-    const __bf16* Ap = sg.A + (long)(rowBase + srow) * 768 + skof;
-    const __bf16* Wp = sg.Wt + (long)(colBase + srow) * 768 + skof;
-    int w = t >> 6, l = t & 63;
-    int wr = (w >> 1) << 5, wc = (w & 1) << 5;
-    int fr = l & 15, g = l >> 4;
-    f32x4 acc[2][2] = {};
-    bf16x8 a0, a1, w0, w1;
-    auto LOADM = [&]() {
-        a0 = *(const bf16x8*)(Ap); a1 = *(const bf16x8*)(Ap + 32);
-        w0 = *(const bf16x8*)(Wp); w1 = *(const bf16x8*)(Wp + 32);
-        Ap += 64; Wp += 64;
-    };
-    LOADM();
-    for (int ks = 0; ks < 12; ks++) {
-        __syncthreads();
-        *(bf16x8*)(&As[srow * LDT + skof]) = a0;
-        *(bf16x8*)(&As[srow * LDT + 32 + skof]) = a1;
-        *(bf16x8*)(&Bs[srow * LDT + skof]) = w0;
-        *(bf16x8*)(&Bs[srow * LDT + 32 + skof]) = w1;
-        if (ks + 1 < 12) LOADM();
-        __syncthreads();
-#pragma unroll
-        for (int sub = 0; sub < 2; sub++) {
-            int ko = sub * 32 + g * 8;
-            bf16x8 fa0 = *(const bf16x8*)(&As[(wr + fr) * LDT + ko]);
-            bf16x8 fa1 = *(const bf16x8*)(&As[(wr + 16 + fr) * LDT + ko]);
-            bf16x8 fb0 = *(const bf16x8*)(&Bs[(wc + fr) * LDT + ko]);
-            bf16x8 fb1 = *(const bf16x8*)(&Bs[(wc + 16 + fr) * LDT + ko]);
-            acc[0][0] = __builtin_amdgcn_mfma_f32_16x16x32_bf16(fa0, fb0, acc[0][0], 0, 0, 0);
-            acc[0][1] = __builtin_amdgcn_mfma_f32_16x16x32_bf16(fa0, fb1, acc[0][1], 0, 0, 0);
-            acc[1][0] = __builtin_amdgcn_mfma_f32_16x16x32_bf16(fa1, fb0, acc[1][0], 0, 0, 0);
-            acc[1][1] = __builtin_amdgcn_mfma_f32_16x16x32_bf16(fa1, fb1, acc[1][1], 0, 0, 0);
-        }
-    }
-#pragma unroll
-    for (int fi = 0; fi < 2; fi++)
-#pragma unroll
-    for (int fj = 0; fj < 2; fj++)
-#pragma unroll
-    for (int r = 0; r < 4; r++) {
-        int row = rowBase + wr + fi * 16 + g * 4 + r;
-        int col = colBase + wc + fj * 16 + (l & 15);
-        if (row < sg.Mtot)
-            sg.Cb[(long)row * sg.ldc + col] = (__bf16)acc[fi][fj][r];
-    }
-}
-
 struct QHSeg {
     const __bf16 *GLh, *GLl, *HYh, *HYl;
     __bf16 *outH, *outL;
@@ -607,9 +568,7 @@
     constexpr int scPad = (XR * YRp * 4 + 15) & ~15;
     constexpr int btSz = 2 * 64 * Cpad * 2;
     constexpr int gOff = btSz;
-    __shared__ alignas(16) char POOL[gOff + 2 * XR * Cpad * 2];
-    __shared__ alignas(16) char POOL2[18432 - (gOff + 2 * XR * Cpad * 2)];
-    (void)POOL2;
+    __shared__ alignas(16) char POOL[18432];
     __bf16* Ah_ = (__bf16*)POOL;
     __bf16* Al_ = Ah_ + XR * LDT;
     int seg = blockIdx.x >> 5, b = blockIdx.x & 31;
@@ -658,9 +617,9 @@
             bf16x8 fal = *(const bf16x8*)(&Al_[(xm * 16 + fr) * LDT + kb]);
             bf16x8 fbh = *(const bf16x8*)(&Bh_[(yc * 16 + fr) * LDT + kb]);
             bf16x8 fbl = *(const bf16x8*)(&Bl_[(yc * 16 + fr) * LDT + kb]);
-            acc = __builtin_amdgcn_mfma_f32_16x16x32_bf16(fah, fbh, acc, 0, 0, 0);
-            acc = __builtin_amdgcn_mfma_f32_16x16x32_bf16(fah, fbl, acc, 0, 0, 0);
-            acc = __builtin_amdgcn_mfma_f32_16x16x32_bf16(fal, fbh, acc, 0, 0, 0);
+            acc = MFMA(fah, fbh, acc, 0, 0, 0);
+            acc = MFMA(fah, fbl, acc, 0, 0, 0);
+            acc = MFMA(fal, fbh, acc, 0, 0, 0);
         }
     }
     __syncthreads();
@@ -710,9 +669,9 @@
         for (int m = 0; m < 2; m++) {
             bf16x8 gah = *(const bf16x8*)(&Gh[(m * 16 + fr) * Cpad + g * 8]);
             bf16x8 gal = *(const bf16x8*)(&Gl[(m * 16 + fr) * Cpad + g * 8]);
-            a2[m] = __builtin_amdgcn_mfma_f32_16x16x32_bf16(gah, bh, a2[m], 0, 0, 0);
-            a2[m] = __builtin_amdgcn_mfma_f32_16x16x32_bf16(gal, bh, a2[m], 0, 0, 0);
-            a2[m] = __builtin_amdgcn_mfma_f32_16x16x32_bf16(gah, blv, a2[m], 0, 0, 0);
+            a2[m] = MFMA(gah, bh, a2[m], 0, 0, 0);
+            a2[m] = MFMA(gal, bh, a2[m], 0, 0, 0);
+            a2[m] = MFMA(gah, blv, a2[m], 0, 0, 0);
         }
 #pragma unroll
         for (int m = 0; m < 2; m++)
@@ -800,9 +759,9 @@
                 bf16x8 fal = *(const bf16x8*)(&Al_[(xm * 16 + fr) * LDT + kb]);
                 bf16x8 fbh = *(const bf16x8*)(&Bh_[(yc * 16 + fr) * LDT + kb]);
                 bf16x8 fbl = *(const bf16x8*)(&Bl_[(yc * 16 + fr) * LDT + kb]);
-                acc[ff] = __builtin_amdgcn_mfma_f32_16x16x32_bf16(fah, fbh, acc[ff], 0, 0, 0);
-                acc[ff] = __builtin_amdgcn_mfma_f32_16x16x32_bf16(fah, fbl, acc[ff], 0, 0, 0);
-                acc[ff] = __builtin_amdgcn_mfma_f32_16x16x32_bf16(fal, fbh, acc[ff], 0, 0, 0);
+                acc[ff] = MFMA(fah, fbh, acc[ff], 0, 0, 0);
+                acc[ff] = MFMA(fah, fbl, acc[ff], 0, 0, 0);
+                acc[ff] = MFMA(fal, fbh, acc[ff], 0, 0, 0);
             }
         }
     }
@@ -857,8 +816,8 @@
             for (int m = 0; m < NM; m++) {
                 bf16x8 gah = *(const bf16x8*)(&Gh[(m * 16 + fr) * Cpad + ks + g * 8]);
                 bf16x8 gal = *(const bf16x8*)(&Gl[(m * 16 + fr) * Cpad + ks + g * 8]);
-                a2[m] = __builtin_amdgcn_mfma_f32_16x16x32_bf16(gah, bh, a2[m], 0, 0, 0);
-                a2[m] = __builtin_amdgcn_mfma_f32_16x16x32_bf16(gal, bh, a2[m], 0, 0, 0);
+                a2[m] = MFMA(gah, bh, a2[m], 0, 0, 0);
+                a2[m] = MFMA(gal, bh, a2[m], 0, 0, 0);
             }
         }
         float mx = 0.f;
@@ -993,8 +952,7 @@
     prep_kernel<<<6336, blk, 0, stream>>>(W5, W6, W7, W8, W9, W10, W11, W12, W13, W14,
                                           W5t_h, W5t_l, WsQT_h, WsQT_l, W6t_h, W6t_l,
                                           W1112T, W78t, W1314t);
-    cvt2n_kernel<<<3072, blk, 0, stream>>>(Ha, Ha_h, Ha_l, ra);
-    cvt2n_kernel<<<1024, blk, 0, stream>>>(Hq, Hq_h, Hq_l, rq);
+    cvt2n_kernel<<<4096, blk, 0, stream>>>(Ha, Ha_h, Ha_l, ra, Hq, Hq_h, Hq_l, rq);
 
     simmax_kernel<<<1024, blk, 0, stream>>>(Hp, Ha_h, Ha_l, Hq_h, Hq_l, ra, rq, amax);
     score_top2_kernel<<<32, dim3(64), 0, stream>>>(amax, topidx);
@@ -1002,16 +960,16 @@
 
     {
         PXArgs pa{};
-        pa.s[0] = { Ha_h, Ha_l, W5t_h, W5t_l, C1_h, C1_l, 3072, 768, 48 };
-        pa.s[1] = { Hq_h, Hq_l, WsQT_h, WsQT_l, HqS_h, HqS_l, 1024, 1536, 16 };
-        pa.s[2] = { Hps_h, Hps_l, WsQT_h, WsQT_l, c1_h, c1_l, 4096, 768, 64 };
-        projx_kernel<<<1728, blk, 0, stream>>>(pa);
+        pa.s[0] = { Ha_h, Ha_l, W5t_h, W5t_l, C1_h, C1_l, 768, 24 };
+        pa.s[1] = { Hq_h, Hq_l, WsQT_h, WsQT_l, HqS_h, HqS_l, 1536, 8 };
+        pa.s[2] = { Hps_h, Hps_l, WsQT_h, WsQT_l, c1_h, c1_l, 768, 32 };
+        projxb_kernel<<<432, blk, 0, stream>>>(pa);
     }
     {
         PPArgs pa{};
-        pa.s[0] = { Hq_h, W1112T, HqS2_bf, 1024, 1536, 16 };
-        pa.s[1] = { Hps_h, W1112T + (long)768 * 768, HpsW12_bf, 4096, 768, 64 };
-        projp_kernel<<<1152, blk, 0, stream>>>(pa);
+        pa.s[0] = { Hq_h, W1112T, HqS2_bf, 1536, 8 };
+        pa.s[1] = { Hps_h, W1112T + (long)768 * 768, HpsW12_bf, 768, 32 };
+        projpb_kernel<<<288, blk, 0, stream>>>(pa);
     }
 
     {
@@ -1031,10 +989,10 @@
         }
         qkh_kernel<<<12 * 32, blk, 0, stream>>>(qa);
     }
-    mgemm3_kernel<1><<<dim3(48, 12), blk, 0, stream>>>(hats_h, hats_l, 2304, 3072, W6t_h, W6t_l, bar, 768, bar_h, nullptr);
+    mgemm3b_kernel<1><<<dim3(24, 6), blk, 0, stream>>>(hats_h, hats_l, 2304, W6t_h, W6t_l, bar, 768, bar_h, nullptr);
     mgemm_gate_kernel<<<dim3(48, 12), blk, 0, stream>>>(bar_h, W78t, b8, Ha, bar, Ho_h, Ho_l);
-    mgemm3_kernel<2><<<dim3(48, 12), blk, 0, stream>>>(Ho_h, Ho_l, 768, 3072, WsQT_h + (long)768 * 768, WsQT_l + (long)768 * 768, nullptr, 768, c4_h, c4_l);
-    mgemm_kernel<0, 1><<<dim3(48, 12), blk, 0, stream>>>(Ho_h, 768, 3072, W1112T, nullptr, nullptr, 768, HoW11_bf);
+    mgemm3b_kernel<2><<<dim3(24, 6), blk, 0, stream>>>(Ho_h, Ho_l, 768, WsQT_h + (long)768 * 768, WsQT_l + (long)768 * 768, nullptr, 768, c4_h, c4_l);
+    mgemmb_kernel<<<dim3(24, 6), blk, 0, stream>>>(Ho_h, 768, W1112T, HoW11_bf, 768);
 
     {
         QSArgs qa{};
```

New measurement: 490.4 us. +10.9%, slower.
